# Performance work log

Hardware: AMD Instinct MI355X
Metric: run time of the kernel (lower is better)

## Reference

```python
import jax, jax.numpy as jnp
import numpy as np

C_S = 384; C_Z = 128; C_RES = 128; H = 12; HD = 32; L = 8; RB = 2; NA = 7
TSF = 10.0; EPS = 1e-8; B = 2; N = 512; NRES = 21


def layernorm(x, g, b, eps=1e-5):
    m = jnp.mean(x, -1, keepdims=True)
    v = jnp.mean((x - m) ** 2, -1, keepdims=True)
    return (x - m) * jax.lax.rsqrt(v + eps) * g + b


def lin(x, w, b=None):
    y = x @ w.T
    return y if b is None else y + b


def rot_vec(R, v):
    return jnp.einsum('...ij,...j->...i', R, v)


def make_rigid(n, ca, c, eps=1e-7):
    # Gram-Schmidt backbone frame construction (openfold make_transform_from_reference)
    t = -ca
    n_xyz = n + t; c_xyz = c + t
    cx, cy, cz = c_xyz[..., 0], c_xyz[..., 1], c_xyz[..., 2]
    z = jnp.zeros_like(cx); o = jnp.ones_like(cx)
    nrm = jnp.sqrt(eps + cx**2 + cy**2)
    s1 = -cy / nrm; c1 = cx / nrm
    R1 = jnp.stack([jnp.stack([c1, -s1, z], -1), jnp.stack([s1, c1, z], -1), jnp.stack([z, z, o], -1)], -2)
    nrm2 = jnp.sqrt(eps + cx**2 + cy**2 + cz**2)
    s2 = cz / nrm2; c2 = jnp.sqrt(cx**2 + cy**2) / nrm2
    R2 = jnp.stack([jnp.stack([c2, z, s2], -1), jnp.stack([z, o, z], -1), jnp.stack([-s2, z, c2], -1)], -2)
    Rc = R2 @ R1
    n2 = rot_vec(Rc, n_xyz)
    ny, nz = n2[..., 1], n2[..., 2]
    nrm3 = jnp.sqrt(eps + ny**2 + nz**2)
    sn = -nz / nrm3; cn = ny / nrm3
    Rn = jnp.stack([jnp.stack([o, z, z], -1), jnp.stack([z, cn, -sn], -1), jnp.stack([z, sn, cn], -1)], -2)
    R = jnp.swapaxes(Rn @ Rc, -1, -2)
    return R, ca


def to4x4(R, t):
    bot = jnp.zeros(R.shape[:-2] + (1, 4), R.dtype).at[..., 0, 3].set(1.0)
    top = jnp.concatenate([R, t[..., None]], -1)
    return jnp.concatenate([top, bot], -2)


def compose(R1, t1, R2, t2):
    return R1 @ R2, rot_vec(R1, t2) + t1


def structure_fwd(s, z, aatype, mask, ln_s_g, ln_s_b, ln_z_g, ln_z_b, w_in, b_in, w_b, b_b,
                  attn_ln_g, attn_ln_b, attn_wqkv, attn_wo, attn_bo, attn_wg, attn_bg,
                  tr_ln_g, tr_ln_b, tr_w1, tr_b1, tr_w2, tr_b2, w_bb, b_bb,
                  ar_win, ar_bin, ar_winit, ar_binit, ar_w1, ar_b1, ar_w2, ar_b2, ar_wout, ar_bout,
                  default_frames, group_idx, atom_mask, lit_positions):
    Bd, Nd = s.shape[:2]
    s = layernorm(s, ln_s_g, ln_s_b)
    s_init = s
    s = lin(s, w_in, b_in)
    zn = layernorm(z, ln_z_g, ln_z_b)
    bmat = lin(zn, w_b, b_b)                                # [B,N,N,L*H]
    bmat = jnp.transpose(bmat, (0, 3, 1, 2)).reshape(Bd, L, H, Nd, Nd)
    key_mask = (mask[:, None, None, :] == 0)
    for i in range(L):
        xn = layernorm(s, attn_ln_g[i], attn_ln_b[i])
        t = lin(xn, attn_wqkv[i]).reshape(Bd, Nd, H, 3 * HD).transpose(0, 2, 1, 3)
        q, k, v = jnp.split(t, 3, axis=-1)                  # each [B,H,N,HD]
        a = jnp.einsum('bhqc,bhkc->bhqk', q * HD ** -0.5, k) + bmat[:, i]
        a = jnp.where(key_mask, -1e9, a)
        a = jax.nn.softmax(a, axis=-1)
        y = jnp.einsum('bhqk,bhkc->bqhc', a, v).reshape(Bd, Nd, C_S)
        g = jax.nn.sigmoid(lin(xn, attn_wg[i], attn_bg[i]))
        s = s + lin(g * y, attn_wo[i], attn_bo[i])
        xt = layernorm(s, tr_ln_g[i], tr_ln_b[i])
        s = s + lin(jax.nn.relu(lin(xt, tr_w1[i], tr_b1[i])), tr_w2[i], tr_b2[i])
    # angle resnet
    a0 = lin(jax.nn.relu(s_init), ar_winit, ar_binit)
    a = lin(jax.nn.relu(s), ar_win, ar_bin) + a0
    for j in range(RB):
        h = lin(jax.nn.relu(a), ar_w1[j], ar_b1[j])
        h = lin(jax.nn.relu(h), ar_w2[j], ar_b2[j])
        a = a + h
    ang = lin(jax.nn.relu(a), ar_wout, ar_bout).reshape(Bd, Nd, NA, 2)
    unnorm = ang
    denom = jnp.sqrt(jnp.maximum(jnp.sum(ang ** 2, -1, keepdims=True), EPS))
    angles = ang / denom
    # backbone rigid from predicted pseudo-atoms
    n_, ca_, c_ = jnp.split(lin(s, w_bb, b_bb), 3, axis=-1)
    Rbb, tbb = make_rigid(n_, ca_, c_)
    tbb = tbb * TSF
    # torsion_angles_to_frames
    d4 = default_frames[aatype]                             # [B,N,8,4,4]
    dR = d4[..., :3, :3]; dt = d4[..., :3, 3]
    bb_sin = jnp.zeros(angles.shape[:-2] + (1,), angles.dtype)
    bb_cos = jnp.ones_like(bb_sin)
    sin_a = jnp.concatenate([bb_sin, angles[..., 0]], -1)   # [B,N,8]
    cos_a = jnp.concatenate([bb_cos, angles[..., 1]], -1)
    z8 = jnp.zeros_like(sin_a); o8 = jnp.ones_like(sin_a)
    Ra = jnp.stack([jnp.stack([o8, z8, z8], -1), jnp.stack([z8, cos_a, -sin_a], -1), jnp.stack([z8, sin_a, cos_a], -1)], -2)
    Rf = dR @ Ra; tf = dt
    R5, t5 = compose(Rf[..., 4, :, :], tf[..., 4, :], Rf[..., 5, :, :], tf[..., 5, :])
    R6, t6 = compose(R5, t5, Rf[..., 6, :, :], tf[..., 6, :])
    R7, t7 = compose(R6, t6, Rf[..., 7, :, :], tf[..., 7, :])
    Rall = jnp.concatenate([Rf[..., :5, :, :], jnp.stack([R5, R6, R7], -3)], -3)
    tall = jnp.concatenate([tf[..., :5, :], jnp.stack([t5, t6, t7], -2)], -2)
    Rg = jnp.einsum('bnij,bngjk->bngik', Rbb, Rall)
    tg = jnp.einsum('bnij,bngj->bngi', Rbb, tall) + tbb[..., None, :]
    # frames + literature positions -> atom14
    oh = jax.nn.one_hot(group_idx[aatype], 8, dtype=Rg.dtype)   # [B,N,14,8]
    Ratom = jnp.einsum('bnag,bngij->bnaij', oh, Rg)
    tatom = jnp.einsum('bnag,bngi->bnai', oh, tg)
    lit = lit_positions[aatype]                             # [B,N,14,3]
    pred = jnp.einsum('bnaij,bnaj->bnai', Ratom, lit) + tatom
    pred = pred * atom_mask[aatype][..., None]
    return angles, unnorm, to4x4(Rbb, tbb), to4x4(Rg, tg), pred, s


def setup_inputs():
    key = jax.random.key(0)
    ks = iter(jax.random.split(key, 64))
    nrm = lambda shape: jax.random.normal(next(ks), shape, jnp.float32) * 0.02
    d = {}
    d['s'] = jax.random.normal(next(ks), (B, N, C_S), jnp.float32)
    d['z'] = jax.random.normal(next(ks), (B, N, N, C_Z), jnp.float32)
    d['aatype'] = jax.random.randint(next(ks), (B, N), 0, NRES)
    d['mask'] = jax.random.randint(next(ks), (B, N), 0, 2).astype(jnp.int32)
    d['ln_s_g'] = jnp.ones(C_S); d['ln_s_b'] = jnp.zeros(C_S)
    d['ln_z_g'] = jnp.ones(C_Z); d['ln_z_b'] = jnp.zeros(C_Z)
    d['w_in'] = nrm((C_S, C_S)); d['b_in'] = jnp.zeros(C_S)
    d['w_b'] = nrm((L * H, C_Z)); d['b_b'] = jnp.zeros(L * H)
    d['attn_ln_g'] = jnp.ones((L, C_S)); d['attn_ln_b'] = jnp.zeros((L, C_S))
    d['attn_wqkv'] = nrm((L, 3 * C_S, C_S))
    d['attn_wo'] = nrm((L, C_S, C_S)); d['attn_bo'] = jnp.zeros((L, C_S))
    d['attn_wg'] = nrm((L, C_S, C_S)); d['attn_bg'] = jnp.ones((L, C_S))
    d['tr_ln_g'] = jnp.ones((L, C_S)); d['tr_ln_b'] = jnp.zeros((L, C_S))
    d['tr_w1'] = nrm((L, C_S, C_S)); d['tr_b1'] = jnp.zeros((L, C_S))
    d['tr_w2'] = nrm((L, C_S, C_S)); d['tr_b2'] = jnp.zeros((L, C_S))
    d['w_bb'] = nrm((9, C_S)); d['b_bb'] = jnp.zeros(9)
    d['ar_win'] = nrm((C_RES, C_S)); d['ar_bin'] = jnp.zeros(C_RES)
    d['ar_winit'] = nrm((C_RES, C_S)); d['ar_binit'] = jnp.zeros(C_RES)
    d['ar_w1'] = nrm((RB, C_RES, C_RES)); d['ar_b1'] = jnp.zeros((RB, C_RES))
    d['ar_w2'] = nrm((RB, C_RES, C_RES)); d['ar_b2'] = jnp.zeros((RB, C_RES))
    d['ar_wout'] = nrm((2 * NA, C_RES)); d['ar_bout'] = jnp.zeros(2 * NA)
    df = jnp.tile(jnp.eye(4, dtype=jnp.float32), (NRES, 8, 1, 1))
    df = df.at[..., :3, 3].set(jax.random.normal(next(ks), (NRES, 8, 3)))
    d['default_frames'] = df
    d['group_idx'] = jax.random.randint(next(ks), (NRES, 14), 0, 8)
    d['atom_mask'] = (jax.random.uniform(next(ks), (NRES, 14)) < 0.9).astype(jnp.float32)
    d['lit_positions'] = jax.random.normal(next(ks), (NRES, 14, 3), jnp.float32)
    return d


def reference(s, z, aatype, mask, ln_s_g, ln_s_b, ln_z_g, ln_z_b, w_in, b_in, w_b, b_b,
              attn_ln_g, attn_ln_b, attn_wqkv, attn_wo, attn_bo, attn_wg, attn_bg,
              tr_ln_g, tr_ln_b, tr_w1, tr_b1, tr_w2, tr_b2, w_bb, b_bb,
              ar_win, ar_bin, ar_winit, ar_binit, ar_w1, ar_b1, ar_w2, ar_b2, ar_wout, ar_bout,
              default_frames, group_idx, atom_mask, lit_positions):
    return structure_fwd(s, z, aatype, mask, ln_s_g, ln_s_b, ln_z_g, ln_z_b, w_in, b_in, w_b, b_b,
                         attn_ln_g, attn_ln_b, attn_wqkv, attn_wo, attn_bo, attn_wg, attn_bg,
                         tr_ln_g, tr_ln_b, tr_w1, tr_b1, tr_w2, tr_b2, w_bb, b_bb,
                         ar_win, ar_bin, ar_winit, ar_binit, ar_w1, ar_b1, ar_w2, ar_b2, ar_wout, ar_bout,
                         default_frames, group_idx, atom_mask, lit_positions)
```

## Files before the change

### kernel.cpp

```cpp
#include <hip/hip_runtime.h>
#include <hip/hip_bf16.h>

typedef __attribute__((ext_vector_type(8))) short bf16x8;
typedef __attribute__((ext_vector_type(4))) float f32x4;
typedef unsigned short u16;

__device__ __forceinline__ u16 f2bf(float f) {
  union { __hip_bfloat16 b; u16 u; } v;
  v.b = __float2bfloat16(f);
  return v.u;
}
__device__ __forceinline__ float bf2f(u16 s) {
  union { unsigned u; float f; } v; v.u = ((unsigned)s) << 16;
  return v.f;
}
__device__ __forceinline__ f32x4 mfma_bf16(bf16x8 a, bf16x8 b, f32x4 c) {
  return __builtin_amdgcn_mfma_f32_16x16x32_bf16(a, b, c, 0, 0, 0);
}
__device__ __forceinline__ void split2(float x, u16& h, u16& l) {
  h = f2bf(x);
  l = f2bf(x - bf2f(h));
}
template <int SPL>
__device__ __forceinline__ void splitN(float x, u16* o) {
  float r = x;
  #pragma unroll
  for (int i = 0; i < SPL; i++) {
    o[i] = f2bf(r);
    if (i + 1 < SPL) r = r - bf2f(o[i]);
  }
}

struct P2 { const float* s; u16* d; int n; };
struct Prep2Args { P2 j[7]; };
__global__ __launch_bounds__(256) void prep2_kernel(Prep2Args A, int total4) {
  for (int i4 = blockIdx.x * 256 + threadIdx.x; i4 < total4; i4 += gridDim.x * 256) {
    int i = i4 * 4;
    #pragma unroll
    for (int jj = 0; jj < 7; jj++) {
      if (i < A.j[jj].n) {
        const float* src = A.j[jj].s;
        u16* dh = A.j[jj].d;
        u16* dl = dh + A.j[jj].n;
        float4 v = *(const float4*)(src + i);
        ushort4 h, l;
        split2(v.x, h.x, l.x); split2(v.y, h.y, l.y);
        split2(v.z, h.z, l.z); split2(v.w, h.w, l.w);
        *(ushort4*)(dh + i) = h;
        *(ushort4*)(dl + i) = l;
        break;
      }
      i -= A.j[jj].n;
    }
  }
}
struct P3 { const float* s; u16* d; int n; };
struct Prep3Args { P3 j[4]; };
__global__ __launch_bounds__(256) void prep3_kernel(Prep3Args A, int total4) {
  for (int i4 = blockIdx.x * 256 + threadIdx.x; i4 < total4; i4 += gridDim.x * 256) {
    int i = i4 * 4;
    #pragma unroll
    for (int jj = 0; jj < 4; jj++) {
      if (i < A.j[jj].n) {
        const float* src = A.j[jj].s;
        u16* d0 = A.j[jj].d;
        u16* d1 = d0 + A.j[jj].n;
        u16* d2 = d1 + A.j[jj].n;
        float4 v = *(const float4*)(src + i);
        float xv[4] = {v.x, v.y, v.z, v.w};
        ushort4 o0, o1, o2;
        u16* po0 = (u16*)&o0; u16* po1 = (u16*)&o1; u16* po2 = (u16*)&o2;
        #pragma unroll
        for (int e = 0; e < 4; e++) {
          u16 tmp[3]; splitN<3>(xv[e], tmp);
          po0[e] = tmp[0]; po1[e] = tmp[1]; po2[e] = tmp[2];
        }
        *(ushort4*)(d0 + i) = o0;
        *(ushort4*)(d1 + i) = o1;
        *(ushort4*)(d2 + i) = o2;
        break;
      }
      i -= A.j[jj].n;
    }
  }
}

__global__ __launch_bounds__(256) void ln_kernel(
    const float* __restrict__ x, const float* __restrict__ gamma,
    const float* __restrict__ beta, float* __restrict__ o, int rows, int C) {
  int wid = threadIdx.x >> 6, lane = threadIdx.x & 63;
  int row = blockIdx.x * 4 + wid;
  if (row >= rows) return;
  const float* xr = x + (size_t)row * C;
  float s = 0.f, s2 = 0.f;
  for (int c = lane; c < C; c += 64) { float v = xr[c]; s += v; s2 += v * v; }
  #pragma unroll
  for (int off = 32; off >= 1; off >>= 1) {
    s += __shfl_xor(s, off);
    s2 += __shfl_xor(s2, off);
  }
  float m = s / C;
  float var = s2 / C - m * m;
  float rs = rsqrtf(var + 1e-5f);
  float* orow = o + (size_t)row * C;
  for (int c = lane; c < C; c += 64) orow[c] = (xr[c] - m) * rs * gamma[c] + beta[c];
}

template <int SPL, int LNA, int INRELU, int ACT, int ACC, int STATS, int OUT2>
__global__ __launch_bounds__(128) void gemm_kernel(
    const float* __restrict__ A, const float* __restrict__ pin,
    const float* __restrict__ lng, const float* __restrict__ lnb,
    const u16* __restrict__ w0p, const u16* __restrict__ w1p, const u16* __restrict__ w2p,
    const float* __restrict__ bias,
    float* __restrict__ O, float* __restrict__ O2, float* __restrict__ pout,
    int M, int N, int K) {
  __shared__ __align__(16) u16 a_pl[SPL][32][40];
  __shared__ __align__(16) u16 w_pl[SPL][64][40];
  const int n0 = blockIdx.x * 64, m0 = blockIdx.y * 32;
  const int t = threadIdx.x;
  const int wid = t >> 6, lane = t & 63;
  const int cl = lane & 15, cg = lane >> 4;
  const int ar = t >> 2, aq = t & 3;
  const int wr = t >> 1, wh2 = t & 1;
  const float* ap = A + (size_t)(m0 + ar) * K + aq * 8;
  const u16* wp[SPL];
  {
    const u16* tmp[3] = {w0p, w1p, w2p};
    #pragma unroll
    for (int p = 0; p < SPL; p++) wp[p] = tmp[p] + (size_t)(n0 + wr) * K + wh2 * 16;
  }
  float rm = 0.f, rrs = 1.f;
  if (LNA) {
    float s = 0.f, s2 = 0.f;
    #pragma unroll
    for (int pq = 0; pq < 6; pq++) {
      s  += pin[(m0 + ar) * 16 + pq * 2];
      s2 += pin[(m0 + ar) * 16 + pq * 2 + 1];
    }
    rm = s * (1.f / 384.f);
    rrs = rsqrtf(s2 * (1.f / 384.f) - rm * rm + 1e-5f);
  }
  float4 ra0, ra1, rg0, rg1, rb0, rb1;
  uint4 rw[SPL][2];
  auto GLOAD = [&](int k0) {
    ra0 = ((const float4*)(ap + k0))[0];
    ra1 = ((const float4*)(ap + k0))[1];
    #pragma unroll
    for (int p = 0; p < SPL; p++) {
      rw[p][0] = *(const uint4*)(wp[p] + k0);
      rw[p][1] = *(const uint4*)(wp[p] + k0 + 8);
    }
    if (LNA) {
      rg0 = ((const float4*)(lng + k0 + aq * 8))[0];
      rg1 = ((const float4*)(lng + k0 + aq * 8))[1];
      rb0 = ((const float4*)(lnb + k0 + aq * 8))[0];
      rb1 = ((const float4*)(lnb + k0 + aq * 8))[1];
    }
  };
  GLOAD(0);
  f32x4 acc[4] = {};
  for (int k0 = 0; k0 < K; k0 += 32) {
    {
      float av[8] = {ra0.x, ra0.y, ra0.z, ra0.w, ra1.x, ra1.y, ra1.z, ra1.w};
      if (LNA) {
        float gv[8] = {rg0.x, rg0.y, rg0.z, rg0.w, rg1.x, rg1.y, rg1.z, rg1.w};
        float bv[8] = {rb0.x, rb0.y, rb0.z, rb0.w, rb1.x, rb1.y, rb1.z, rb1.w};
        #pragma unroll
        for (int j = 0; j < 8; j++) av[j] = (av[j] - rm) * rrs * gv[j] + bv[j];
      }
      if (INRELU) {
        #pragma unroll
        for (int j = 0; j < 8; j++) av[j] = fmaxf(av[j], 0.f);
      }
      union { u16 s[8]; uint4 u; } pk[SPL];
      #pragma unroll
      for (int j = 0; j < 8; j++) {
        u16 tmp[SPL]; splitN<SPL>(av[j], tmp);
        #pragma unroll
        for (int p = 0; p < SPL; p++) pk[p].s[j] = tmp[p];
      }
      #pragma unroll
      for (int p = 0; p < SPL; p++) *(uint4*)&a_pl[p][ar][aq * 8] = pk[p].u;
      #pragma unroll
      for (int p = 0; p < SPL; p++) {
        *(uint4*)&w_pl[p][wr][wh2 * 16] = rw[p][0];
        *(uint4*)&w_pl[p][wr][wh2 * 16 + 8] = rw[p][1];
      }
    }
    __syncthreads();
    if (k0 + 32 < K) GLOAD(k0 + 32);
    bf16x8 av[SPL];
    #pragma unroll
    for (int p = 0; p < SPL; p++) av[p] = *(const bf16x8*)&a_pl[p][wid * 16 + cl][cg * 8];
    bf16x8 bv[SPL][4];
    #pragma unroll
    for (int p = 0; p < SPL; p++)
      #pragma unroll
      for (int nt = 0; nt < 4; nt++)
        bv[p][nt] = *(const bf16x8*)&w_pl[p][nt * 16 + cl][cg * 8];
    #pragma unroll
    for (int d = 0; d < SPL; d++)
      #pragma unroll
      for (int i2 = 0; i2 <= d; i2++) {
        #pragma unroll
        for (int nt = 0; nt < 4; nt++)
          acc[nt] = mfma_bf16(av[i2], bv[d - i2][nt], acc[nt]);
      }
    __syncthreads();
  }
  float ps[4], ps2[4];
  #pragma unroll
  for (int i = 0; i < 4; i++) { ps[i] = 0.f; ps2[i] = 0.f; }
  #pragma unroll
  for (int nt = 0; nt < 4; nt++) {
    #pragma unroll
    for (int i = 0; i < 4; i++) {
      int r = m0 + wid * 16 + cg * 4 + i;
      int c = n0 + nt * 16 + cl;
      float v = acc[nt][i];
      if (bias) v += bias[c];
      if (ACT == 1) v = fmaxf(v, 0.f);
      if (ACT == 2) v = 1.f / (1.f + __expf(-v));
      size_t oi = (size_t)r * N + c;
      float nv = ACC ? (O[oi] + v) : v;
      O[oi] = nv;
      if (OUT2) O2[oi] = nv;
      if (STATS) { ps[i] += nv; ps2[i] += nv * nv; }
    }
  }
  if (STATS) {
    #pragma unroll
    for (int i = 0; i < 4; i++) {
      #pragma unroll
      for (int off = 1; off < 16; off <<= 1) {
        ps[i] += __shfl_xor(ps[i], off);
        ps2[i] += __shfl_xor(ps2[i], off);
      }
    }
    if (cl == 0) {
      #pragma unroll
      for (int i = 0; i < 4; i++) {
        int r = m0 + wid * 16 + cg * 4 + i;
        pout[r * 16 + blockIdx.x * 2] = ps[i];
        pout[r * 16 + blockIdx.x * 2 + 1] = ps2[i];
      }
    }
  }
}

__global__ __launch_bounds__(128) void gemm_qkvg_kernel(
    const float* __restrict__ A, const float* __restrict__ pin,
    const float* __restrict__ lng, const float* __restrict__ lnb,
    const u16* __restrict__ wqh, const u16* __restrict__ wql,
    const u16* __restrict__ wgh, const u16* __restrict__ wgl,
    const float* __restrict__ bg,
    u16* __restrict__ qkvh, u16* __restrict__ qkvl, float* __restrict__ gbuf) {
  __shared__ __align__(16) u16 a_pl[2][32][40];
  __shared__ __align__(16) u16 w_pl[2][64][40];
  const int n0 = blockIdx.x * 64, m0 = blockIdx.y * 32;
  const bool isg = (n0 >= 1152);
  const int t = threadIdx.x;
  const int wid = t >> 6, lane = t & 63;
  const int cl = lane & 15, cg = lane >> 4;
  const int ar = t >> 2, aq = t & 3;
  const int wr = t >> 1, wh2 = t & 1;
  const float* ap = A + (size_t)(m0 + ar) * 384 + aq * 8;
  const u16* wph = (isg ? wgh + (size_t)(n0 - 1152 + wr) * 384 : wqh + (size_t)(n0 + wr) * 384) + wh2 * 16;
  const u16* wpl = (isg ? wgl + (size_t)(n0 - 1152 + wr) * 384 : wql + (size_t)(n0 + wr) * 384) + wh2 * 16;
  float s = 0.f, s2 = 0.f;
  #pragma unroll
  for (int pq = 0; pq < 6; pq++) {
    s  += pin[(m0 + ar) * 16 + pq * 2];
    s2 += pin[(m0 + ar) * 16 + pq * 2 + 1];
  }
  const float rm = s * (1.f / 384.f);
  const float rrs = rsqrtf(s2 * (1.f / 384.f) - rm * rm + 1e-5f);
  float4 ra0, ra1, rg0, rg1, rb0, rb1;
  uint4 rwh0, rwh1, rwl0, rwl1;
  auto GLOAD = [&](int k0) {
    ra0 = ((const float4*)(ap + k0))[0];
    ra1 = ((const float4*)(ap + k0))[1];
    rwh0 = *(const uint4*)(wph + k0);
    rwh1 = *(const uint4*)(wph + k0 + 8);
    rwl0 = *(const uint4*)(wpl + k0);
    rwl1 = *(const uint4*)(wpl + k0 + 8);
    rg0 = ((const float4*)(lng + k0 + aq * 8))[0];
    rg1 = ((const float4*)(lng + k0 + aq * 8))[1];
    rb0 = ((const float4*)(lnb + k0 + aq * 8))[0];
    rb1 = ((const float4*)(lnb + k0 + aq * 8))[1];
  };
  GLOAD(0);
  f32x4 acc[4] = {};
  for (int k0 = 0; k0 < 384; k0 += 32) {
    {
      float av[8] = {ra0.x, ra0.y, ra0.z, ra0.w, ra1.x, ra1.y, ra1.z, ra1.w};
      float gv[8] = {rg0.x, rg0.y, rg0.z, rg0.w, rg1.x, rg1.y, rg1.z, rg1.w};
      float bv[8] = {rb0.x, rb0.y, rb0.z, rb0.w, rb1.x, rb1.y, rb1.z, rb1.w};
      union { u16 s[8]; uint4 u; } ph, pl;
      #pragma unroll
      for (int j = 0; j < 8; j++) {
        float x = (av[j] - rm) * rrs * gv[j] + bv[j];
        split2(x, ph.s[j], pl.s[j]);
      }
      *(uint4*)&a_pl[0][ar][aq * 8] = ph.u;
      *(uint4*)&a_pl[1][ar][aq * 8] = pl.u;
      *(uint4*)&w_pl[0][wr][wh2 * 16] = rwh0;
      *(uint4*)&w_pl[0][wr][wh2 * 16 + 8] = rwh1;
      *(uint4*)&w_pl[1][wr][wh2 * 16] = rwl0;
      *(uint4*)&w_pl[1][wr][wh2 * 16 + 8] = rwl1;
    }
    __syncthreads();
    if (k0 + 32 < 384) GLOAD(k0 + 32);
    bf16x8 ah = *(const bf16x8*)&a_pl[0][wid * 16 + cl][cg * 8];
    bf16x8 al = *(const bf16x8*)&a_pl[1][wid * 16 + cl][cg * 8];
    bf16x8 bh[4], bl[4];
    #pragma unroll
    for (int nt = 0; nt < 4; nt++) {
      bh[nt] = *(const bf16x8*)&w_pl[0][nt * 16 + cl][cg * 8];
      bl[nt] = *(const bf16x8*)&w_pl[1][nt * 16 + cl][cg * 8];
    }
    #pragma unroll
    for (int nt = 0; nt < 4; nt++) acc[nt] = mfma_bf16(ah, bh[nt], acc[nt]);
    #pragma unroll
    for (int nt = 0; nt < 4; nt++) acc[nt] = mfma_bf16(ah, bl[nt], acc[nt]);
    #pragma unroll
    for (int nt = 0; nt < 4; nt++) acc[nt] = mfma_bf16(al, bh[nt], acc[nt]);
    __syncthreads();
  }
  #pragma unroll
  for (int nt = 0; nt < 4; nt++) {
    #pragma unroll
    for (int i = 0; i < 4; i++) {
      int r = m0 + wid * 16 + cg * 4 + i;
      int c = n0 + nt * 16 + cl;
      float v = acc[nt][i];
      if (isg) {
        int cc = c - 1152;
        v = 1.f / (1.f + __expf(-(v + bg[cc])));
        gbuf[(size_t)r * 384 + cc] = v;
      } else {
        u16 hh, ll; split2(v, hh, ll);
        qkvh[(size_t)r * 1152 + c] = hh;
        qkvl[(size_t)r * 1152 + c] = ll;
      }
    }
  }
}

__global__ __launch_bounds__(512) void zbmat_kernel(
    const float* __restrict__ z, const float* __restrict__ gamma,
    const float* __restrict__ beta, const u16* __restrict__ wbh,
    const u16* __restrict__ wbl, const float* __restrict__ bbias,
    float* __restrict__ bm) {
  __shared__ __align__(16) u16 w_h[96][136], w_l[96][136];
  __shared__ __align__(16) u16 a_h[2][64][136], a_l[2][64][136];
  const int b = blockIdx.x >> 9;
  const int i = blockIdx.x & 511;
  const int t = threadIdx.x;
  for (int idx = t; idx < 1536; idx += 512) {
    int r2 = idx >> 4, c2 = (idx & 15) * 8;
    *(uint4*)&w_h[r2][c2] = *(const uint4*)(wbh + r2 * 128 + c2);
    *(uint4*)&w_l[r2][c2] = *(const uint4*)(wbl + r2 * 128 + c2);
  }
  const int r = t >> 3, q = t & 7;
  const int cq = q * 16;
  const float* zbase = z + ((size_t)(b * 512 + i) * 512) * 128 + (size_t)r * 128 + cq;
  float4 gv[4], bv[4];
  #pragma unroll
  for (int ii = 0; ii < 4; ii++) {
    gv[ii] = *(const float4*)(gamma + cq + ii * 4);
    bv[ii] = *(const float4*)(beta + cq + ii * 4);
  }
  const int wid = t >> 6, lane = t & 63;
  const int cl = lane & 15, cg = lane >> 4;
  const int m = wid & 3, g = wid >> 2;
  const int arow = m * 16 + cl;
  float bb[3];
  #pragma unroll
  for (int nt = 0; nt < 3; nt++) bb[nt] = bbias[(g * 3 + nt) * 16 + cl];
  float4 v[4];

  auto ln_store = [&](int dst) {
    float s = 0.f, s2 = 0.f;
    #pragma unroll
    for (int ii = 0; ii < 4; ii++) {
      s += v[ii].x + v[ii].y + v[ii].z + v[ii].w;
      s2 += v[ii].x * v[ii].x + v[ii].y * v[ii].y + v[ii].z * v[ii].z + v[ii].w * v[ii].w;
    }
    s += __shfl_xor(s, 1); s2 += __shfl_xor(s2, 1);
    s += __shfl_xor(s, 2); s2 += __shfl_xor(s2, 2);
    s += __shfl_xor(s, 4); s2 += __shfl_xor(s2, 4);
    const float mu = s * (1.f / 128.f);
    const float var = s2 * (1.f / 128.f) - mu * mu;
    const float rs = rsqrtf(var + 1e-5f);
    float xv[16];
    #pragma unroll
    for (int w2 = 0; w2 < 4; w2++) {
      float4 x = v[w2], g2 = gv[w2], be = bv[w2];
      xv[w2 * 4 + 0] = (x.x - mu) * rs * g2.x + be.x;
      xv[w2 * 4 + 1] = (x.y - mu) * rs * g2.y + be.y;
      xv[w2 * 4 + 2] = (x.z - mu) * rs * g2.z + be.z;
      xv[w2 * 4 + 3] = (x.w - mu) * rs * g2.w + be.w;
    }
    union { u16 s[8]; uint4 u; } ph, pl;
    #pragma unroll
    for (int j = 0; j < 8; j++) split2(xv[j], ph.s[j], pl.s[j]);
    *(uint4*)&a_h[dst][r][cq] = ph.u;
    *(uint4*)&a_l[dst][r][cq] = pl.u;
    #pragma unroll
    for (int j = 0; j < 8; j++) split2(xv[8 + j], ph.s[j], pl.s[j]);
    *(uint4*)&a_h[dst][r][cq + 8] = ph.u;
    *(uint4*)&a_l[dst][r][cq + 8] = pl.u;
  };

  #pragma unroll
  for (int ii = 0; ii < 4; ii++) v[ii] = ((const float4*)zbase)[ii];
  ln_store(0);
  __syncthreads();

  int cur = 0;
  for (int jt = 0; jt < 8; jt++) {
    if (jt < 7) {
      const float* src = zbase + (size_t)(jt + 1) * 64 * 128;
      #pragma unroll
      for (int ii = 0; ii < 4; ii++) v[ii] = ((const float4*)src)[ii];
    }
    f32x4 acc[3] = {};
    #pragma unroll
    for (int ks = 0; ks < 4; ks++) {
      bf16x8 ah = *(const bf16x8*)&a_h[cur][arow][ks * 32 + cg * 8];
      bf16x8 al = *(const bf16x8*)&a_l[cur][arow][ks * 32 + cg * 8];
      bf16x8 bh[3], bl[3];
      #pragma unroll
      for (int nt = 0; nt < 3; nt++) {
        bh[nt] = *(const bf16x8*)&w_h[(g * 3 + nt) * 16 + cl][ks * 32 + cg * 8];
        bl[nt] = *(const bf16x8*)&w_l[(g * 3 + nt) * 16 + cl][ks * 32 + cg * 8];
      }
      #pragma unroll
      for (int nt = 0; nt < 3; nt++) acc[nt] = mfma_bf16(ah, bh[nt], acc[nt]);
      #pragma unroll
      for (int nt = 0; nt < 3; nt++) acc[nt] = mfma_bf16(ah, bl[nt], acc[nt]);
      #pragma unroll
      for (int nt = 0; nt < 3; nt++) acc[nt] = mfma_bf16(al, bh[nt], acc[nt]);
    }
    #pragma unroll
    for (int nt = 0; nt < 3; nt++) {
      float4 o;
      o.x = acc[nt][0] + bb[nt]; o.y = acc[nt][1] + bb[nt];
      o.z = acc[nt][2] + bb[nt]; o.w = acc[nt][3] + bb[nt];
      int ch = (g * 3 + nt) * 16 + cl;
      *(float4*)&bm[((size_t)(b * 96 + ch) * 512 + i) * 512 + jt * 64 + m * 16 + cg * 4] = o;
    }
    if (jt < 7) ln_store(cur ^ 1);
    __syncthreads();
    cur ^= 1;
  }
}

__global__ __launch_bounds__(128) void attn_kernel(
    const u16* __restrict__ qkvh, const u16* __restrict__ qkvl,
    const float* __restrict__ bmat, const int* __restrict__ maskp,
    const float* __restrict__ gate, float* __restrict__ ybuf, int layer) {
  __shared__ __align__(16) u16 vT_h[32][522];
  __shared__ __align__(16) u16 vT_l[32][522];
  __shared__ __align__(16) u16 pst_h[2][16][36];
  __shared__ __align__(16) u16 pst_l[2][16][36];
  const int bid = blockIdx.x;
  const int qb = bid & 15;
  const int hh = (bid >> 4) % 12;
  const int b = bid / 192;
  const int q0 = qb * 32;
  const int t = threadIdx.x;
  const int wid = t >> 6;
  const int lane = t & 63;
  const int cl = lane & 15, cg = lane >> 4;

  for (int idx = t; idx < 2048; idx += 128) {
    int k = idx >> 2, c8 = (idx & 3) * 8;
    size_t off = (size_t)(b * 512 + k) * 1152 + hh * 96 + 64 + c8;
    union { uint4 u; u16 s[8]; } vh, vl;
    vh.u = *(const uint4*)(qkvh + off);
    vl.u = *(const uint4*)(qkvl + off);
    #pragma unroll
    for (int j = 0; j < 8; j++) {
      vT_h[c8 + j][k] = vh.s[j];
      vT_l[c8 + j][k] = vl.s[j];
    }
  }

  const int qrow = q0 + wid * 16 + cl;
  const size_t qoff = (size_t)(b * 512 + qrow) * 1152 + hh * 96 + cg * 8;
  bf16x8 qh = *(const bf16x8*)(qkvh + qoff);
  bf16x8 ql = *(const bf16x8*)(qkvl + qoff);

  __syncthreads();

  const f32x4 zero4 = {0.f, 0.f, 0.f, 0.f};
  const float qs = 0.17677669529663687f;
  f32x4 sc[32];
  #pragma unroll
  for (int nt = 0; nt < 32; nt++) {
    int kk = nt * 16 + cl;
    size_t koff = (size_t)(b * 512 + kk) * 1152 + hh * 96 + 32 + cg * 8;
    bf16x8 kh = *(const bf16x8*)(qkvh + koff);
    bf16x8 kl = *(const bf16x8*)(qkvl + koff);
    f32x4 a = mfma_bf16(qh, kh, zero4);
    a = mfma_bf16(qh, kl, a);
    a = mfma_bf16(ql, kh, a);
    sc[nt] = a;
  }

  const size_t bc = (size_t)(b * 96 + layer * 12 + hh);
  #pragma unroll
  for (int nt = 0; nt < 32; nt++) {
    int kk = nt * 16 + cl;
    int mk = maskp[b * 512 + kk];
    #pragma unroll
    for (int i2 = 0; i2 < 4; i2++) {
      int qq = q0 + wid * 16 + cg * 4 + i2;
      float bias = bmat[(bc * 512 + qq) * 512 + kk];
      float vv = sc[nt][i2] * qs + bias;
      sc[nt][i2] = (mk == 0) ? -1e9f : vv;
    }
  }

  float inv[4];
  #pragma unroll
  for (int i2 = 0; i2 < 4; i2++) {
    float mx = -3e38f;
    #pragma unroll
    for (int nt = 0; nt < 32; nt++) mx = fmaxf(mx, sc[nt][i2]);
    mx = fmaxf(mx, __shfl_xor(mx, 1));
    mx = fmaxf(mx, __shfl_xor(mx, 2));
    mx = fmaxf(mx, __shfl_xor(mx, 4));
    mx = fmaxf(mx, __shfl_xor(mx, 8));
    float ss = 0.f;
    #pragma unroll
    for (int nt = 0; nt < 32; nt++) {
      float p = __expf(sc[nt][i2] - mx);
      sc[nt][i2] = p;
      ss += p;
    }
    ss += __shfl_xor(ss, 1);
    ss += __shfl_xor(ss, 2);
    ss += __shfl_xor(ss, 4);
    ss += __shfl_xor(ss, 8);
    inv[i2] = 1.f / ss;
  }

  f32x4 yacc[2] = {};
  for (int ks = 0; ks < 16; ks++) {
    #pragma unroll
    for (int half = 0; half < 2; half++) {
      int nt = ks * 2 + half;
      #pragma unroll
      for (int i2 = 0; i2 < 4; i2++) {
        u16 h2, l2; split2(sc[nt][i2] * inv[i2], h2, l2);
        pst_h[wid][cg * 4 + i2][half * 16 + cl] = h2;
        pst_l[wid][cg * 4 + i2][half * 16 + cl] = l2;
      }
    }
    __syncthreads();
    bf16x8 ph = *(const bf16x8*)&pst_h[wid][cl][cg * 8];
    bf16x8 pl = *(const bf16x8*)&pst_l[wid][cl][cg * 8];
    #pragma unroll
    for (int nt2 = 0; nt2 < 2; nt2++) {
      bf16x8 vh = *(const bf16x8*)&vT_h[nt2 * 16 + cl][ks * 32 + cg * 8];
      bf16x8 vl = *(const bf16x8*)&vT_l[nt2 * 16 + cl][ks * 32 + cg * 8];
      yacc[nt2] = mfma_bf16(ph, vh, yacc[nt2]);
      yacc[nt2] = mfma_bf16(ph, vl, yacc[nt2]);
      yacc[nt2] = mfma_bf16(pl, vh, yacc[nt2]);
    }
    __syncthreads();
  }

  #pragma unroll
  for (int nt2 = 0; nt2 < 2; nt2++) {
    #pragma unroll
    for (int i2 = 0; i2 < 4; i2++) {
      int qq = q0 + wid * 16 + cg * 4 + i2;
      int c = nt2 * 16 + cl;
      size_t oi = (size_t)(b * 512 + qq) * 384 + hh * 32 + c;
      ybuf[oi] = yacc[nt2][i2] * gate[oi];
    }
  }
}

template <int NOUT, int K, int RELU>
__global__ __launch_bounds__(256) void proj_kernel(
    const float* __restrict__ A, const float* __restrict__ W,
    const float* __restrict__ bias, float* __restrict__ O) {
  const int wid = threadIdx.x >> 6, lane = threadIdx.x & 63;
  const int row = blockIdx.x * 4 + wid;
  const float* a = A + (size_t)row * K;
  float av[K / 64];
  #pragma unroll
  for (int j = 0; j < K / 64; j++) {
    float v = a[lane + 64 * j];
    av[j] = RELU ? fmaxf(v, 0.f) : v;
  }
  float res = 0.f;
  #pragma unroll
  for (int n = 0; n < NOUT; n++) {
    float s = 0.f;
    #pragma unroll
    for (int j = 0; j < K / 64; j++) s += av[j] * W[n * K + lane + 64 * j];
    #pragma unroll
    for (int off = 32; off >= 1; off >>= 1) s += __shfl_xor(s, off);
    if (lane == n) res = s + bias[n];
  }
  if (lane < NOUT) O[(size_t)row * NOUT + lane] = res;
}

__device__ __forceinline__ void m3m(float* o, const float* a, const float* b) {
  #pragma unroll
  for (int i = 0; i < 3; i++)
    #pragma unroll
    for (int j = 0; j < 3; j++)
      o[i * 3 + j] = a[i * 3 + 0] * b[0 * 3 + j] + a[i * 3 + 1] * b[1 * 3 + j] + a[i * 3 + 2] * b[2 * 3 + j];
}
__device__ __forceinline__ void m3v(float* o, const float* a, const float* v) {
  #pragma unroll
  for (int i = 0; i < 3; i++)
    o[i] = a[i * 3 + 0] * v[0] + a[i * 3 + 1] * v[1] + a[i * 3 + 2] * v[2];
}

__global__ __launch_bounds__(256) void tail_kernel(
    const float* __restrict__ angraw, const float* __restrict__ bbbuf,
    const int* __restrict__ aatype, const float* __restrict__ deff,
    const int* __restrict__ gidx, const float* __restrict__ amask,
    const float* __restrict__ lit,
    float* __restrict__ o_ang, float* __restrict__ o_un,
    float* __restrict__ o_bb4, float* __restrict__ o_rg4, float* __restrict__ o_pred) {
  int idx = blockIdx.x * 256 + threadIdx.x;
  if (idx >= 1024) return;
  float ang[14];
  #pragma unroll
  for (int a = 0; a < 7; a++) {
    float s0 = angraw[idx * 14 + a * 2], s1 = angraw[idx * 14 + a * 2 + 1];
    o_un[(idx * 7 + a) * 2] = s0; o_un[(idx * 7 + a) * 2 + 1] = s1;
    float d = sqrtf(fmaxf(s0 * s0 + s1 * s1, 1e-8f));
    ang[a * 2] = s0 / d; ang[a * 2 + 1] = s1 / d;
    o_ang[(idx * 7 + a) * 2] = ang[a * 2]; o_ang[(idx * 7 + a) * 2 + 1] = ang[a * 2 + 1];
  }
  const float* p = bbbuf + (size_t)idx * 9;
  float nx = p[0] - p[3], ny = p[1] - p[4], nz = p[2] - p[5];
  float cx = p[6] - p[3], cy = p[7] - p[4], cz = p[8] - p[5];
  const float eps = 1e-7f;
  float nrm = sqrtf(eps + cx * cx + cy * cy);
  float s1 = -cy / nrm, c1 = cx / nrm;
  float nrm2 = sqrtf(eps + cx * cx + cy * cy + cz * cz);
  float s2 = cz / nrm2, c2 = sqrtf(cx * cx + cy * cy) / nrm2;
  float Rc[9] = { c2 * c1, -c2 * s1, s2,
                  s1,      c1,       0.f,
                  -s2 * c1, s2 * s1, c2 };
  float n2y = Rc[3] * nx + Rc[4] * ny + Rc[5] * nz;
  float n2z = Rc[6] * nx + Rc[7] * ny + Rc[8] * nz;
  float nrm3 = sqrtf(eps + n2y * n2y + n2z * n2z);
  float sn = -n2z / nrm3, cn = n2y / nrm3;
  float Rm[9];
  Rm[0] = Rc[0]; Rm[1] = Rc[1]; Rm[2] = Rc[2];
  Rm[3] = cn * Rc[3] - sn * Rc[6];
  Rm[4] = cn * Rc[4] - sn * Rc[7];
  Rm[5] = cn * Rc[5] - sn * Rc[8];
  Rm[6] = sn * Rc[3] + cn * Rc[6];
  Rm[7] = sn * Rc[4] + cn * Rc[7];
  Rm[8] = sn * Rc[5] + cn * Rc[8];
  float Rb[9] = { Rm[0], Rm[3], Rm[6],
                  Rm[1], Rm[4], Rm[7],
                  Rm[2], Rm[5], Rm[8] };
  float tb[3] = { p[3] * 10.f, p[4] * 10.f, p[5] * 10.f };
  {
    float* o = o_bb4 + (size_t)idx * 16;
    o[0] = Rb[0]; o[1] = Rb[1]; o[2] = Rb[2]; o[3] = tb[0];
    o[4] = Rb[3]; o[5] = Rb[4]; o[6] = Rb[5]; o[7] = tb[1];
    o[8] = Rb[6]; o[9] = Rb[7]; o[10] = Rb[8]; o[11] = tb[2];
    o[12] = 0.f; o[13] = 0.f; o[14] = 0.f; o[15] = 1.f;
  }
  int aa = aatype[idx];
  float Rf[8][9], tf[8][3];
  for (int g = 0; g < 8; g++) {
    const float* d4 = deff + ((size_t)aa * 8 + g) * 16;
    float sa = 0.f, ca = 1.f;
    if (g > 0) { sa = ang[(g - 1) * 2]; ca = ang[(g - 1) * 2 + 1]; }
    #pragma unroll
    for (int i = 0; i < 3; i++) {
      float d0 = d4[i * 4 + 0], d1 = d4[i * 4 + 1], d2 = d4[i * 4 + 2];
      Rf[g][i * 3 + 0] = d0;
      Rf[g][i * 3 + 1] = d1 * ca + d2 * sa;
      Rf[g][i * 3 + 2] = -d1 * sa + d2 * ca;
      tf[g][i] = d4[i * 4 + 3];
    }
  }
  float Rall[8][9], tall[8][3];
  for (int g = 0; g < 5; g++) {
    #pragma unroll
    for (int i = 0; i < 9; i++) Rall[g][i] = Rf[g][i];
    #pragma unroll
    for (int i = 0; i < 3; i++) tall[g][i] = tf[g][i];
  }
  m3m(Rall[5], Rf[4], Rf[5]); m3v(tall[5], Rf[4], tf[5]);
  tall[5][0] += tf[4][0]; tall[5][1] += tf[4][1]; tall[5][2] += tf[4][2];
  m3m(Rall[6], Rall[5], Rf[6]); m3v(tall[6], Rall[5], tf[6]);
  tall[6][0] += tall[5][0]; tall[6][1] += tall[5][1]; tall[6][2] += tall[5][2];
  m3m(Rall[7], Rall[6], Rf[7]); m3v(tall[7], Rall[6], tf[7]);
  tall[7][0] += tall[6][0]; tall[7][1] += tall[6][1]; tall[7][2] += tall[6][2];
  float RG[8][9], TG[8][3];
  for (int g = 0; g < 8; g++) {
    m3m(RG[g], Rb, Rall[g]);
    m3v(TG[g], Rb, tall[g]);
    TG[g][0] += tb[0]; TG[g][1] += tb[1]; TG[g][2] += tb[2];
    float* o = o_rg4 + ((size_t)idx * 8 + g) * 16;
    o[0] = RG[g][0]; o[1] = RG[g][1]; o[2] = RG[g][2]; o[3] = TG[g][0];
    o[4] = RG[g][3]; o[5] = RG[g][4]; o[6] = RG[g][5]; o[7] = TG[g][1];
    o[8] = RG[g][6]; o[9] = RG[g][7]; o[10] = RG[g][8]; o[11] = TG[g][2];
    o[12] = 0.f; o[13] = 0.f; o[14] = 0.f; o[15] = 1.f;
  }
  for (int a = 0; a < 14; a++) {
    int gi = gidx[aa * 14 + a];
    const float* lp = lit + ((size_t)aa * 14 + a) * 3;
    float mk = amask[aa * 14 + a];
    float px = RG[gi][0] * lp[0] + RG[gi][1] * lp[1] + RG[gi][2] * lp[2] + TG[gi][0];
    float py = RG[gi][3] * lp[0] + RG[gi][4] * lp[1] + RG[gi][5] * lp[2] + TG[gi][1];
    float pz = RG[gi][6] * lp[0] + RG[gi][7] * lp[1] + RG[gi][8] * lp[2] + TG[gi][2];
    float* op = o_pred + ((size_t)idx * 14 + a) * 3;
    op[0] = px * mk; op[1] = py * mk; op[2] = pz * mk;
  }
}

extern "C" void kernel_launch(void* const* d_in, const int* in_sizes, int n_in,
                              void* d_out, int out_size, void* d_ws, size_t ws_size,
                              hipStream_t stream) {
  (void)in_sizes; (void)n_in; (void)out_size; (void)ws_size;
  const float* s_in    = (const float*)d_in[0];
  const float* z_in    = (const float*)d_in[1];
  const int*   aatype  = (const int*)d_in[2];
  const int*   maskp   = (const int*)d_in[3];
  const float* ln_s_g  = (const float*)d_in[4];
  const float* ln_s_b  = (const float*)d_in[5];
  const float* ln_z_g  = (const float*)d_in[6];
  const float* ln_z_b  = (const float*)d_in[7];
  const float* w_in    = (const float*)d_in[8];
  const float* b_in    = (const float*)d_in[9];
  const float* w_b     = (const float*)d_in[10];
  const float* b_b     = (const float*)d_in[11];
  const float* attn_ln_g = (const float*)d_in[12];
  const float* attn_ln_b = (const float*)d_in[13];
  const float* attn_wqkv = (const float*)d_in[14];
  const float* attn_wo   = (const float*)d_in[15];
  const float* attn_bo   = (const float*)d_in[16];
  const float* attn_wg   = (const float*)d_in[17];
  const float* attn_bg   = (const float*)d_in[18];
  const float* tr_ln_g   = (const float*)d_in[19];
  const float* tr_ln_b   = (const float*)d_in[20];
  const float* tr_w1     = (const float*)d_in[21];
  const float* tr_b1     = (const float*)d_in[22];
  const float* tr_w2     = (const float*)d_in[23];
  const float* tr_b2     = (const float*)d_in[24];
  const float* w_bb      = (const float*)d_in[25];
  const float* b_bb      = (const float*)d_in[26];
  const float* ar_win    = (const float*)d_in[27];
  const float* ar_bin    = (const float*)d_in[28];
  const float* ar_winit  = (const float*)d_in[29];
  const float* ar_binit  = (const float*)d_in[30];
  const float* ar_w1     = (const float*)d_in[31];
  const float* ar_b1     = (const float*)d_in[32];
  const float* ar_w2     = (const float*)d_in[33];
  const float* ar_b2     = (const float*)d_in[34];
  const float* ar_wout   = (const float*)d_in[35];
  const float* ar_bout   = (const float*)d_in[36];
  const float* def_frames= (const float*)d_in[37];
  const int*   group_idx = (const int*)d_in[38];
  const float* atom_mask = (const float*)d_in[39];
  const float* lit_pos   = (const float*)d_in[40];

  char* p = (char*)d_ws;
  float* bmat   = (float*)p;          p += 201326592;
  float* s_init = (float*)p;          p += 1572864;
  float* s_cur  = (float*)p;          p += 1572864;
  u16*   qkvh   = (u16*)p;            p += 2359296;
  u16*   qkvl   = (u16*)p;            p += 2359296;
  float* gbuf   = (float*)p;          p += 1572864;
  float* ybuf   = (float*)p;          p += 1572864;
  float* h1buf  = (float*)p;          p += 1572864;
  float* abuf   = (float*)p;          p += 524288;
  float* htmp   = (float*)p;          p += 524288;
  float* pbuf   = (float*)p;          p += 65536;
  float* bbbuf  = (float*)p;          p += 36864;
  float* angraw = (float*)p;          p += 57344;
  u16* ps_qkvw  = (u16*)p;            p += 14155776;
  u16* ps_wg    = (u16*)p;            p += 4718592;
  u16* ps_wo    = (u16*)p;            p += 4718592;
  u16* ps_tr1   = (u16*)p;            p += 4718592;
  u16* ps_tr2   = (u16*)p;            p += 4718592;
  u16* ps_win   = (u16*)p;            p += 589824;
  u16* ps_wb    = (u16*)p;            p += 49152;
  u16* ps_arwin = (u16*)p;            p += 294912;
  u16* ps_arwinit = (u16*)p;          p += 294912;
  u16* ps_arw1  = (u16*)p;            p += 196608;
  u16* ps_arw2  = (u16*)p;            p += 196608;

  float* out    = (float*)d_out;
  float* o_ang  = out;
  float* o_un   = out + 14336;
  float* o_bb4  = out + 28672;
  float* o_rg4  = out + 45056;
  float* o_pred = out + 176128;
  float* o_s    = out + 219136;

  Prep2Args p2;
  p2.j[0] = {attn_wqkv, ps_qkvw, 3538944};
  p2.j[1] = {attn_wg,   ps_wg,   1179648};
  p2.j[2] = {attn_wo,   ps_wo,   1179648};
  p2.j[3] = {tr_w1,     ps_tr1,  1179648};
  p2.j[4] = {tr_w2,     ps_tr2,  1179648};
  p2.j[5] = {w_in,      ps_win,  147456};
  p2.j[6] = {w_b,       ps_wb,   12288};
  prep2_kernel<<<2048, 256, 0, stream>>>(p2, 2104320);
  Prep3Args p3;
  p3.j[0] = {ar_win,   ps_arwin,   49152};
  p3.j[1] = {ar_winit, ps_arwinit, 49152};
  p3.j[2] = {ar_w1,    ps_arw1,    32768};
  p3.j[3] = {ar_w2,    ps_arw2,    32768};
  prep3_kernel<<<160, 256, 0, stream>>>(p3, 40960);

  ln_kernel<<<256, 256, 0, stream>>>(s_in, ln_s_g, ln_s_b, s_init, 1024, 384);
  gemm_kernel<2, 0, 0, 0, 0, 1, 0><<<dim3(6, 32), 128, 0, stream>>>(
      s_init, nullptr, nullptr, nullptr, ps_win, ps_win + 147456, nullptr,
      b_in, s_cur, nullptr, pbuf, 1024, 384, 384);
  zbmat_kernel<<<1024, 512, 0, stream>>>(z_in, ln_z_g, ln_z_b, ps_wb, ps_wb + 12288, b_b, bmat);

  for (int l = 0; l < 8; ++l) {
    gemm_qkvg_kernel<<<dim3(24, 32), 128, 0, stream>>>(
        s_cur, pbuf, attn_ln_g + l * 384, attn_ln_b + l * 384,
        ps_qkvw + (size_t)l * 442368, ps_qkvw + 3538944 + (size_t)l * 442368,
        ps_wg + (size_t)l * 147456, ps_wg + 1179648 + (size_t)l * 147456,
        attn_bg + l * 384, qkvh, qkvl, gbuf);
    attn_kernel<<<384, 128, 0, stream>>>(qkvh, qkvl, bmat, maskp, gbuf, ybuf, l);
    gemm_kernel<2, 0, 0, 0, 1, 1, 0><<<dim3(6, 32), 128, 0, stream>>>(
        ybuf, nullptr, nullptr, nullptr,
        ps_wo + (size_t)l * 147456, ps_wo + 1179648 + (size_t)l * 147456, nullptr,
        attn_bo + l * 384, s_cur, nullptr, pbuf, 1024, 384, 384);
    gemm_kernel<2, 1, 0, 1, 0, 0, 0><<<dim3(6, 32), 128, 0, stream>>>(
        s_cur, pbuf, tr_ln_g + l * 384, tr_ln_b + l * 384,
        ps_tr1 + (size_t)l * 147456, ps_tr1 + 1179648 + (size_t)l * 147456, nullptr,
        tr_b1 + l * 384, h1buf, nullptr, nullptr, 1024, 384, 384);
    if (l < 7)
      gemm_kernel<2, 0, 0, 0, 1, 1, 0><<<dim3(6, 32), 128, 0, stream>>>(
          h1buf, nullptr, nullptr, nullptr,
          ps_tr2 + (size_t)l * 147456, ps_tr2 + 1179648 + (size_t)l * 147456, nullptr,
          tr_b2 + l * 384, s_cur, nullptr, pbuf, 1024, 384, 384);
    else
      gemm_kernel<2, 0, 0, 0, 1, 1, 1><<<dim3(6, 32), 128, 0, stream>>>(
          h1buf, nullptr, nullptr, nullptr,
          ps_tr2 + (size_t)l * 147456, ps_tr2 + 1179648 + (size_t)l * 147456, nullptr,
          tr_b2 + l * 384, s_cur, o_s, pbuf, 1024, 384, 384);
  }

  gemm_kernel<3, 0, 1, 0, 0, 0, 0><<<dim3(2, 32), 128, 0, stream>>>(
      s_cur, nullptr, nullptr, nullptr,
      ps_arwin, ps_arwin + 49152, ps_arwin + 98304,
      ar_bin, abuf, nullptr, nullptr, 1024, 128, 384);
  gemm_kernel<3, 0, 1, 0, 1, 0, 0><<<dim3(2, 32), 128, 0, stream>>>(
      s_init, nullptr, nullptr, nullptr,
      ps_arwinit, ps_arwinit + 49152, ps_arwinit + 98304,
      ar_binit, abuf, nullptr, nullptr, 1024, 128, 384);
  for (int j = 0; j < 2; ++j) {
    gemm_kernel<3, 0, 1, 0, 0, 0, 0><<<dim3(2, 32), 128, 0, stream>>>(
        abuf, nullptr, nullptr, nullptr,
        ps_arw1 + j * 16384, ps_arw1 + 32768 + j * 16384, ps_arw1 + 65536 + j * 16384,
        ar_b1 + j * 128, htmp, nullptr, nullptr, 1024, 128, 128);
    gemm_kernel<3, 0, 1, 0, 1, 0, 0><<<dim3(2, 32), 128, 0, stream>>>(
        htmp, nullptr, nullptr, nullptr,
        ps_arw2 + j * 16384, ps_arw2 + 32768 + j * 16384, ps_arw2 + 65536 + j * 16384,
        ar_b2 + j * 128, abuf, nullptr, nullptr, 1024, 128, 128);
  }

  proj_kernel<9, 384, 0><<<256, 256, 0, stream>>>(s_cur, w_bb, b_bb, bbbuf);
  proj_kernel<14, 128, 1><<<256, 256, 0, stream>>>(abuf, ar_wout, ar_bout, angraw);
  tail_kernel<<<4, 256, 0, stream>>>(angraw, bbbuf, aatype, def_frames, group_idx,
                                     atom_mask, lit_pos, o_ang, o_un, o_bb4, o_rg4, o_pred);
}
```

Measured before the change: 1.098 ms.

## Double GEMM K-step, restructure pair-bias kernel, fuse angle resnet and tail

The generic and QKVG GEMM kernels now stage 64-wide K tiles in shared memory instead of 32, halving the barrier count per tile. The pair-bias kernel is rewritten to load z rows straight into MFMA fragments in registers and do LayerNorm there, dropping the shared-memory A staging. The angle-resnet GEMMs, the two projection kernels and the tail kernel are merged into one 32-block kernel, which removes about nine launches and their intermediate buffers. The costs are more shared memory per block, and a fused tail that runs on only 32 blocks and may be serialised.

```diff
diff --git a/kernel.cpp b/kernel.cpp
--- a/kernel.cpp
+++ b/kernel.cpp
@@ -114,20 +114,20 @@
     const float* __restrict__ bias,
     float* __restrict__ O, float* __restrict__ O2, float* __restrict__ pout,
     int M, int N, int K) {
-  __shared__ __align__(16) u16 a_pl[SPL][32][40];
-  __shared__ __align__(16) u16 w_pl[SPL][64][40];
+  __shared__ __align__(16) u16 a_pl[SPL][32][72];
+  __shared__ __align__(16) u16 w_pl[SPL][64][72];
   const int n0 = blockIdx.x * 64, m0 = blockIdx.y * 32;
   const int t = threadIdx.x;
   const int wid = t >> 6, lane = t & 63;
   const int cl = lane & 15, cg = lane >> 4;
   const int ar = t >> 2, aq = t & 3;
   const int wr = t >> 1, wh2 = t & 1;
-  const float* ap = A + (size_t)(m0 + ar) * K + aq * 8;
-  const u16* wp[SPL];
+  const float* ap = A + (size_t)(m0 + ar) * K + aq * 16;
+  const u16* wp[3] = {nullptr, nullptr, nullptr};
   {
     const u16* tmp[3] = {w0p, w1p, w2p};
     #pragma unroll
-    for (int p = 0; p < SPL; p++) wp[p] = tmp[p] + (size_t)(n0 + wr) * K + wh2 * 16;
+    for (int p = 0; p < SPL; p++) wp[p] = tmp[p] + (size_t)(n0 + wr) * K + wh2 * 32;
   }
   float rm = 0.f, rrs = 1.f;
   if (LNA) {
@@ -140,72 +140,84 @@
     rm = s * (1.f / 384.f);
     rrs = rsqrtf(s2 * (1.f / 384.f) - rm * rm + 1e-5f);
   }
-  float4 ra0, ra1, rg0, rg1, rb0, rb1;
-  uint4 rw[SPL][2];
+  float4 ra[4], rg[4], rb4[4];
+  uint4 rw[SPL][4];
   auto GLOAD = [&](int k0) {
-    ra0 = ((const float4*)(ap + k0))[0];
-    ra1 = ((const float4*)(ap + k0))[1];
-    #pragma unroll
-    for (int p = 0; p < SPL; p++) {
-      rw[p][0] = *(const uint4*)(wp[p] + k0);
-      rw[p][1] = *(const uint4*)(wp[p] + k0 + 8);
-    }
+    #pragma unroll
+    for (int e = 0; e < 4; e++) ra[e] = ((const float4*)(ap + k0))[e];
+    #pragma unroll
+    for (int p = 0; p < SPL; p++)
+      #pragma unroll
+      for (int e = 0; e < 4; e++) rw[p][e] = *(const uint4*)(wp[p] + k0 + e * 8);
     if (LNA) {
-      rg0 = ((const float4*)(lng + k0 + aq * 8))[0];
-      rg1 = ((const float4*)(lng + k0 + aq * 8))[1];
-      rb0 = ((const float4*)(lnb + k0 + aq * 8))[0];
-      rb1 = ((const float4*)(lnb + k0 + aq * 8))[1];
+      #pragma unroll
+      for (int e = 0; e < 4; e++) {
+        rg[e]  = ((const float4*)(lng + k0 + aq * 16))[e];
+        rb4[e] = ((const float4*)(lnb + k0 + aq * 16))[e];
+      }
     }
   };
   GLOAD(0);
   f32x4 acc[4] = {};
-  for (int k0 = 0; k0 < K; k0 += 32) {
+  for (int k0 = 0; k0 < K; k0 += 64) {
     {
-      float av[8] = {ra0.x, ra0.y, ra0.z, ra0.w, ra1.x, ra1.y, ra1.z, ra1.w};
+      float av[16];
+      #pragma unroll
+      for (int e = 0; e < 4; e++) {
+        av[e * 4 + 0] = ra[e].x; av[e * 4 + 1] = ra[e].y;
+        av[e * 4 + 2] = ra[e].z; av[e * 4 + 3] = ra[e].w;
+      }
       if (LNA) {
-        float gv[8] = {rg0.x, rg0.y, rg0.z, rg0.w, rg1.x, rg1.y, rg1.z, rg1.w};
-        float bv[8] = {rb0.x, rb0.y, rb0.z, rb0.w, rb1.x, rb1.y, rb1.z, rb1.w};
-        #pragma unroll
-        for (int j = 0; j < 8; j++) av[j] = (av[j] - rm) * rrs * gv[j] + bv[j];
+        #pragma unroll
+        for (int e = 0; e < 4; e++) {
+          av[e * 4 + 0] = (av[e * 4 + 0] - rm) * rrs * rg[e].x + rb4[e].x;
+          av[e * 4 + 1] = (av[e * 4 + 1] - rm) * rrs * rg[e].y + rb4[e].y;
+          av[e * 4 + 2] = (av[e * 4 + 2] - rm) * rrs * rg[e].z + rb4[e].z;
+          av[e * 4 + 3] = (av[e * 4 + 3] - rm) * rrs * rg[e].w + rb4[e].w;
+        }
       }
       if (INRELU) {
         #pragma unroll
-        for (int j = 0; j < 8; j++) av[j] = fmaxf(av[j], 0.f);
-      }
-      union { u16 s[8]; uint4 u; } pk[SPL];
-      #pragma unroll
-      for (int j = 0; j < 8; j++) {
+        for (int j = 0; j < 16; j++) av[j] = fmaxf(av[j], 0.f);
+      }
+      u16 sh[SPL][16];
+      #pragma unroll
+      for (int j = 0; j < 16; j++) {
         u16 tmp[SPL]; splitN<SPL>(av[j], tmp);
         #pragma unroll
-        for (int p = 0; p < SPL; p++) pk[p].s[j] = tmp[p];
-      }
-      #pragma unroll
-      for (int p = 0; p < SPL; p++) *(uint4*)&a_pl[p][ar][aq * 8] = pk[p].u;
+        for (int p = 0; p < SPL; p++) sh[p][j] = tmp[p];
+      }
       #pragma unroll
       for (int p = 0; p < SPL; p++) {
-        *(uint4*)&w_pl[p][wr][wh2 * 16] = rw[p][0];
-        *(uint4*)&w_pl[p][wr][wh2 * 16 + 8] = rw[p][1];
+        *(uint4*)&a_pl[p][ar][aq * 16]     = *(const uint4*)&sh[p][0];
+        *(uint4*)&a_pl[p][ar][aq * 16 + 8] = *(const uint4*)&sh[p][8];
+        #pragma unroll
+        for (int e = 0; e < 4; e++) *(uint4*)&w_pl[p][wr][wh2 * 32 + e * 8] = rw[p][e];
       }
     }
     __syncthreads();
-    if (k0 + 32 < K) GLOAD(k0 + 32);
-    bf16x8 av[SPL];
-    #pragma unroll
-    for (int p = 0; p < SPL; p++) av[p] = *(const bf16x8*)&a_pl[p][wid * 16 + cl][cg * 8];
-    bf16x8 bv[SPL][4];
-    #pragma unroll
-    for (int p = 0; p < SPL; p++)
-      #pragma unroll
-      for (int nt = 0; nt < 4; nt++)
-        bv[p][nt] = *(const bf16x8*)&w_pl[p][nt * 16 + cl][cg * 8];
-    #pragma unroll
-    for (int d = 0; d < SPL; d++)
-      #pragma unroll
-      for (int i2 = 0; i2 <= d; i2++) {
+    if (k0 + 64 < K) GLOAD(k0 + 64);
+    #pragma unroll
+    for (int ks2 = 0; ks2 < 2; ks2++) {
+      bf16x8 av_[SPL];
+      #pragma unroll
+      for (int p = 0; p < SPL; p++)
+        av_[p] = *(const bf16x8*)&a_pl[p][wid * 16 + cl][ks2 * 32 + cg * 8];
+      bf16x8 bv[SPL][4];
+      #pragma unroll
+      for (int p = 0; p < SPL; p++)
         #pragma unroll
         for (int nt = 0; nt < 4; nt++)
-          acc[nt] = mfma_bf16(av[i2], bv[d - i2][nt], acc[nt]);
-      }
+          bv[p][nt] = *(const bf16x8*)&w_pl[p][nt * 16 + cl][ks2 * 32 + cg * 8];
+      #pragma unroll
+      for (int d = 0; d < SPL; d++)
+        #pragma unroll
+        for (int i2 = 0; i2 <= d; i2++) {
+          #pragma unroll
+          for (int nt = 0; nt < 4; nt++)
+            acc[nt] = mfma_bf16(av_[i2], bv[d - i2][nt], acc[nt]);
+        }
+    }
     __syncthreads();
   }
   float ps[4], ps2[4];
@@ -255,8 +267,8 @@
     const u16* __restrict__ wgh, const u16* __restrict__ wgl,
     const float* __restrict__ bg,
     u16* __restrict__ qkvh, u16* __restrict__ qkvl, float* __restrict__ gbuf) {
-  __shared__ __align__(16) u16 a_pl[2][32][40];
-  __shared__ __align__(16) u16 w_pl[2][64][40];
+  __shared__ __align__(16) u16 a_pl[2][32][72];
+  __shared__ __align__(16) u16 w_pl[2][64][72];
   const int n0 = blockIdx.x * 64, m0 = blockIdx.y * 32;
   const bool isg = (n0 >= 1152);
   const int t = threadIdx.x;
@@ -264,9 +276,9 @@
   const int cl = lane & 15, cg = lane >> 4;
   const int ar = t >> 2, aq = t & 3;
   const int wr = t >> 1, wh2 = t & 1;
-  const float* ap = A + (size_t)(m0 + ar) * 384 + aq * 8;
-  const u16* wph = (isg ? wgh + (size_t)(n0 - 1152 + wr) * 384 : wqh + (size_t)(n0 + wr) * 384) + wh2 * 16;
-  const u16* wpl = (isg ? wgl + (size_t)(n0 - 1152 + wr) * 384 : wql + (size_t)(n0 + wr) * 384) + wh2 * 16;
+  const float* ap = A + (size_t)(m0 + ar) * 384 + aq * 16;
+  const u16* wph = (isg ? wgh + (size_t)(n0 - 1152 + wr) * 384 : wqh + (size_t)(n0 + wr) * 384) + wh2 * 32;
+  const u16* wpl = (isg ? wgl + (size_t)(n0 - 1152 + wr) * 384 : wql + (size_t)(n0 + wr) * 384) + wh2 * 32;
   float s = 0.f, s2 = 0.f;
   #pragma unroll
   for (int pq = 0; pq < 6; pq++) {
@@ -275,56 +287,63 @@
   }
   const float rm = s * (1.f / 384.f);
   const float rrs = rsqrtf(s2 * (1.f / 384.f) - rm * rm + 1e-5f);
-  float4 ra0, ra1, rg0, rg1, rb0, rb1;
-  uint4 rwh0, rwh1, rwl0, rwl1;
+  float4 ra[4], rg[4], rb4[4];
+  uint4 rwh[4], rwl[4];
   auto GLOAD = [&](int k0) {
-    ra0 = ((const float4*)(ap + k0))[0];
-    ra1 = ((const float4*)(ap + k0))[1];
-    rwh0 = *(const uint4*)(wph + k0);
-    rwh1 = *(const uint4*)(wph + k0 + 8);
-    rwl0 = *(const uint4*)(wpl + k0);
-    rwl1 = *(const uint4*)(wpl + k0 + 8);
-    rg0 = ((const float4*)(lng + k0 + aq * 8))[0];
-    rg1 = ((const float4*)(lng + k0 + aq * 8))[1];
-    rb0 = ((const float4*)(lnb + k0 + aq * 8))[0];
-    rb1 = ((const float4*)(lnb + k0 + aq * 8))[1];
+    #pragma unroll
+    for (int e = 0; e < 4; e++) {
+      ra[e]  = ((const float4*)(ap + k0))[e];
+      rwh[e] = *(const uint4*)(wph + k0 + e * 8);
+      rwl[e] = *(const uint4*)(wpl + k0 + e * 8);
+      rg[e]  = ((const float4*)(lng + k0 + aq * 16))[e];
+      rb4[e] = ((const float4*)(lnb + k0 + aq * 16))[e];
+    }
   };
   GLOAD(0);
   f32x4 acc[4] = {};
-  for (int k0 = 0; k0 < 384; k0 += 32) {
+  for (int k0 = 0; k0 < 384; k0 += 64) {
     {
-      float av[8] = {ra0.x, ra0.y, ra0.z, ra0.w, ra1.x, ra1.y, ra1.z, ra1.w};
-      float gv[8] = {rg0.x, rg0.y, rg0.z, rg0.w, rg1.x, rg1.y, rg1.z, rg1.w};
-      float bv[8] = {rb0.x, rb0.y, rb0.z, rb0.w, rb1.x, rb1.y, rb1.z, rb1.w};
-      union { u16 s[8]; uint4 u; } ph, pl;
-      #pragma unroll
-      for (int j = 0; j < 8; j++) {
-        float x = (av[j] - rm) * rrs * gv[j] + bv[j];
-        split2(x, ph.s[j], pl.s[j]);
-      }
-      *(uint4*)&a_pl[0][ar][aq * 8] = ph.u;
-      *(uint4*)&a_pl[1][ar][aq * 8] = pl.u;
-      *(uint4*)&w_pl[0][wr][wh2 * 16] = rwh0;
-      *(uint4*)&w_pl[0][wr][wh2 * 16 + 8] = rwh1;
-      *(uint4*)&w_pl[1][wr][wh2 * 16] = rwl0;
-      *(uint4*)&w_pl[1][wr][wh2 * 16 + 8] = rwl1;
+      u16 sh[2][16];
+      #pragma unroll
+      for (int e = 0; e < 4; e++) {
+        float xv[4];
+        xv[0] = (ra[e].x - rm) * rrs * rg[e].x + rb4[e].x;
+        xv[1] = (ra[e].y - rm) * rrs * rg[e].y + rb4[e].y;
+        xv[2] = (ra[e].z - rm) * rrs * rg[e].z + rb4[e].z;
+        xv[3] = (ra[e].w - rm) * rrs * rg[e].w + rb4[e].w;
+        #pragma unroll
+        for (int j = 0; j < 4; j++) split2(xv[j], sh[0][e * 4 + j], sh[1][e * 4 + j]);
+      }
+      #pragma unroll
+      for (int p = 0; p < 2; p++) {
+        *(uint4*)&a_pl[p][ar][aq * 16]     = *(const uint4*)&sh[p][0];
+        *(uint4*)&a_pl[p][ar][aq * 16 + 8] = *(const uint4*)&sh[p][8];
+      }
+      #pragma unroll
+      for (int e = 0; e < 4; e++) {
+        *(uint4*)&w_pl[0][wr][wh2 * 32 + e * 8] = rwh[e];
+        *(uint4*)&w_pl[1][wr][wh2 * 32 + e * 8] = rwl[e];
+      }
     }
     __syncthreads();
-    if (k0 + 32 < 384) GLOAD(k0 + 32);
-    bf16x8 ah = *(const bf16x8*)&a_pl[0][wid * 16 + cl][cg * 8];
-    bf16x8 al = *(const bf16x8*)&a_pl[1][wid * 16 + cl][cg * 8];
-    bf16x8 bh[4], bl[4];
-    #pragma unroll
-    for (int nt = 0; nt < 4; nt++) {
-      bh[nt] = *(const bf16x8*)&w_pl[0][nt * 16 + cl][cg * 8];
-      bl[nt] = *(const bf16x8*)&w_pl[1][nt * 16 + cl][cg * 8];
-    }
-    #pragma unroll
-    for (int nt = 0; nt < 4; nt++) acc[nt] = mfma_bf16(ah, bh[nt], acc[nt]);
-    #pragma unroll
-    for (int nt = 0; nt < 4; nt++) acc[nt] = mfma_bf16(ah, bl[nt], acc[nt]);
-    #pragma unroll
-    for (int nt = 0; nt < 4; nt++) acc[nt] = mfma_bf16(al, bh[nt], acc[nt]);
+    if (k0 + 64 < 384) GLOAD(k0 + 64);
+    #pragma unroll
+    for (int ks2 = 0; ks2 < 2; ks2++) {
+      bf16x8 ah = *(const bf16x8*)&a_pl[0][wid * 16 + cl][ks2 * 32 + cg * 8];
+      bf16x8 al = *(const bf16x8*)&a_pl[1][wid * 16 + cl][ks2 * 32 + cg * 8];
+      bf16x8 bh[4], bl[4];
+      #pragma unroll
+      for (int nt = 0; nt < 4; nt++) {
+        bh[nt] = *(const bf16x8*)&w_pl[0][nt * 16 + cl][ks2 * 32 + cg * 8];
+        bl[nt] = *(const bf16x8*)&w_pl[1][nt * 16 + cl][ks2 * 32 + cg * 8];
+      }
+      #pragma unroll
+      for (int nt = 0; nt < 4; nt++) acc[nt] = mfma_bf16(ah, bh[nt], acc[nt]);
+      #pragma unroll
+      for (int nt = 0; nt < 4; nt++) acc[nt] = mfma_bf16(ah, bl[nt], acc[nt]);
+      #pragma unroll
+      for (int nt = 0; nt < 4; nt++) acc[nt] = mfma_bf16(al, bh[nt], acc[nt]);
+    }
     __syncthreads();
   }
   #pragma unroll
@@ -353,107 +372,81 @@
     const u16* __restrict__ wbl, const float* __restrict__ bbias,
     float* __restrict__ bm) {
   __shared__ __align__(16) u16 w_h[96][136], w_l[96][136];
-  __shared__ __align__(16) u16 a_h[2][64][136], a_l[2][64][136];
-  const int b = blockIdx.x >> 9;
-  const int i = blockIdx.x & 511;
+  const int b = blockIdx.x >> 9, i = blockIdx.x & 511;
   const int t = threadIdx.x;
   for (int idx = t; idx < 1536; idx += 512) {
     int r2 = idx >> 4, c2 = (idx & 15) * 8;
     *(uint4*)&w_h[r2][c2] = *(const uint4*)(wbh + r2 * 128 + c2);
     *(uint4*)&w_l[r2][c2] = *(const uint4*)(wbl + r2 * 128 + c2);
   }
-  const int r = t >> 3, q = t & 7;
-  const int cq = q * 16;
-  const float* zbase = z + ((size_t)(b * 512 + i) * 512) * 128 + (size_t)r * 128 + cq;
-  float4 gv[4], bv[4];
-  #pragma unroll
-  for (int ii = 0; ii < 4; ii++) {
-    gv[ii] = *(const float4*)(gamma + cq + ii * 4);
-    bv[ii] = *(const float4*)(beta + cq + ii * 4);
-  }
-  const int wid = t >> 6, lane = t & 63;
+  const int w = t >> 6, lane = t & 63;
   const int cl = lane & 15, cg = lane >> 4;
-  const int m = wid & 3, g = wid >> 2;
-  const int arow = m * 16 + cl;
-  float bb[3];
-  #pragma unroll
-  for (int nt = 0; nt < 3; nt++) bb[nt] = bbias[(g * 3 + nt) * 16 + cl];
-  float4 v[4];
-
-  auto ln_store = [&](int dst) {
+  float bb[6];
+  #pragma unroll
+  for (int nt = 0; nt < 6; nt++) bb[nt] = bbias[nt * 16 + cl];
+  float4 gv[8], bv[8];
+  #pragma unroll
+  for (int ks = 0; ks < 4; ks++) {
+    gv[ks * 2]     = *(const float4*)(gamma + ks * 32 + cg * 8);
+    gv[ks * 2 + 1] = *(const float4*)(gamma + ks * 32 + cg * 8 + 4);
+    bv[ks * 2]     = *(const float4*)(beta + ks * 32 + cg * 8);
+    bv[ks * 2 + 1] = *(const float4*)(beta + ks * 32 + cg * 8 + 4);
+  }
+  __syncthreads();
+  const float* zb = z + ((size_t)(b * 512 + i) * 512) * 128;
+  for (int it = 0; it < 4; it++) {
+    const int j0 = it * 128 + w * 16;
+    const float* zr = zb + (size_t)(j0 + cl) * 128 + cg * 8;
+    float4 v[8];
+    #pragma unroll
+    for (int ks = 0; ks < 4; ks++) {
+      v[ks * 2]     = *(const float4*)(zr + ks * 32);
+      v[ks * 2 + 1] = *(const float4*)(zr + ks * 32 + 4);
+    }
     float s = 0.f, s2 = 0.f;
     #pragma unroll
-    for (int ii = 0; ii < 4; ii++) {
-      s += v[ii].x + v[ii].y + v[ii].z + v[ii].w;
-      s2 += v[ii].x * v[ii].x + v[ii].y * v[ii].y + v[ii].z * v[ii].z + v[ii].w * v[ii].w;
-    }
-    s += __shfl_xor(s, 1); s2 += __shfl_xor(s2, 1);
-    s += __shfl_xor(s, 2); s2 += __shfl_xor(s2, 2);
-    s += __shfl_xor(s, 4); s2 += __shfl_xor(s2, 4);
+    for (int e = 0; e < 8; e++) {
+      s  += v[e].x + v[e].y + v[e].z + v[e].w;
+      s2 += v[e].x * v[e].x + v[e].y * v[e].y + v[e].z * v[e].z + v[e].w * v[e].w;
+    }
+    s += __shfl_xor(s, 16); s2 += __shfl_xor(s2, 16);
+    s += __shfl_xor(s, 32); s2 += __shfl_xor(s2, 32);
     const float mu = s * (1.f / 128.f);
-    const float var = s2 * (1.f / 128.f) - mu * mu;
-    const float rs = rsqrtf(var + 1e-5f);
-    float xv[16];
-    #pragma unroll
-    for (int w2 = 0; w2 < 4; w2++) {
-      float4 x = v[w2], g2 = gv[w2], be = bv[w2];
-      xv[w2 * 4 + 0] = (x.x - mu) * rs * g2.x + be.x;
-      xv[w2 * 4 + 1] = (x.y - mu) * rs * g2.y + be.y;
-      xv[w2 * 4 + 2] = (x.z - mu) * rs * g2.z + be.z;
-      xv[w2 * 4 + 3] = (x.w - mu) * rs * g2.w + be.w;
-    }
-    union { u16 s[8]; uint4 u; } ph, pl;
-    #pragma unroll
-    for (int j = 0; j < 8; j++) split2(xv[j], ph.s[j], pl.s[j]);
-    *(uint4*)&a_h[dst][r][cq] = ph.u;
-    *(uint4*)&a_l[dst][r][cq] = pl.u;
-    #pragma unroll
-    for (int j = 0; j < 8; j++) split2(xv[8 + j], ph.s[j], pl.s[j]);
-    *(uint4*)&a_h[dst][r][cq + 8] = ph.u;
-    *(uint4*)&a_l[dst][r][cq + 8] = pl.u;
-  };
-
-  #pragma unroll
-  for (int ii = 0; ii < 4; ii++) v[ii] = ((const float4*)zbase)[ii];
-  ln_store(0);
-  __syncthreads();
-
-  int cur = 0;
-  for (int jt = 0; jt < 8; jt++) {
-    if (jt < 7) {
-      const float* src = zbase + (size_t)(jt + 1) * 64 * 128;
-      #pragma unroll
-      for (int ii = 0; ii < 4; ii++) v[ii] = ((const float4*)src)[ii];
-    }
-    f32x4 acc[3] = {};
+    const float rs = rsqrtf(s2 * (1.f / 128.f) - mu * mu + 1e-5f);
+    bf16x8 ah[4], al[4];
     #pragma unroll
     for (int ks = 0; ks < 4; ks++) {
-      bf16x8 ah = *(const bf16x8*)&a_h[cur][arow][ks * 32 + cg * 8];
-      bf16x8 al = *(const bf16x8*)&a_l[cur][arow][ks * 32 + cg * 8];
-      bf16x8 bh[3], bl[3];
-      #pragma unroll
-      for (int nt = 0; nt < 3; nt++) {
-        bh[nt] = *(const bf16x8*)&w_h[(g * 3 + nt) * 16 + cl][ks * 32 + cg * 8];
-        bl[nt] = *(const bf16x8*)&w_l[(g * 3 + nt) * 16 + cl][ks * 32 + cg * 8];
-      }
-      #pragma unroll
-      for (int nt = 0; nt < 3; nt++) acc[nt] = mfma_bf16(ah, bh[nt], acc[nt]);
-      #pragma unroll
-      for (int nt = 0; nt < 3; nt++) acc[nt] = mfma_bf16(ah, bl[nt], acc[nt]);
-      #pragma unroll
-      for (int nt = 0; nt < 3; nt++) acc[nt] = mfma_bf16(al, bh[nt], acc[nt]);
-    }
-    #pragma unroll
-    for (int nt = 0; nt < 3; nt++) {
+      union { u16 s[8]; bf16x8 v8; } ph, pl;
+      float xv[8] = {v[ks*2].x, v[ks*2].y, v[ks*2].z, v[ks*2].w,
+                     v[ks*2+1].x, v[ks*2+1].y, v[ks*2+1].z, v[ks*2+1].w};
+      float gg[8] = {gv[ks*2].x, gv[ks*2].y, gv[ks*2].z, gv[ks*2].w,
+                     gv[ks*2+1].x, gv[ks*2+1].y, gv[ks*2+1].z, gv[ks*2+1].w};
+      float be[8] = {bv[ks*2].x, bv[ks*2].y, bv[ks*2].z, bv[ks*2].w,
+                     bv[ks*2+1].x, bv[ks*2+1].y, bv[ks*2+1].z, bv[ks*2+1].w};
+      #pragma unroll
+      for (int e = 0; e < 8; e++) split2((xv[e] - mu) * rs * gg[e] + be[e], ph.s[e], pl.s[e]);
+      ah[ks] = ph.v8; al[ks] = pl.v8;
+    }
+    f32x4 acc[6] = {};
+    #pragma unroll
+    for (int ks = 0; ks < 4; ks++) {
+      #pragma unroll
+      for (int nt = 0; nt < 6; nt++) {
+        bf16x8 bh = *(const bf16x8*)&w_h[nt * 16 + cl][ks * 32 + cg * 8];
+        bf16x8 bl = *(const bf16x8*)&w_l[nt * 16 + cl][ks * 32 + cg * 8];
+        acc[nt] = mfma_bf16(ah[ks], bh, acc[nt]);
+        acc[nt] = mfma_bf16(ah[ks], bl, acc[nt]);
+        acc[nt] = mfma_bf16(al[ks], bh, acc[nt]);
+      }
+    }
+    #pragma unroll
+    for (int nt = 0; nt < 6; nt++) {
       float4 o;
       o.x = acc[nt][0] + bb[nt]; o.y = acc[nt][1] + bb[nt];
       o.z = acc[nt][2] + bb[nt]; o.w = acc[nt][3] + bb[nt];
-      int ch = (g * 3 + nt) * 16 + cl;
-      *(float4*)&bm[((size_t)(b * 96 + ch) * 512 + i) * 512 + jt * 64 + m * 16 + cg * 4] = o;
-    }
-    if (jt < 7) ln_store(cur ^ 1);
-    __syncthreads();
-    cur ^= 1;
+      int ch = nt * 16 + cl;
+      *(float4*)&bm[((size_t)(b * 96 + ch) * 512 + i) * 512 + j0 + cg * 4] = o;
+    }
   }
 }
 
@@ -586,32 +579,6 @@
   }
 }
 
-template <int NOUT, int K, int RELU>
-__global__ __launch_bounds__(256) void proj_kernel(
-    const float* __restrict__ A, const float* __restrict__ W,
-    const float* __restrict__ bias, float* __restrict__ O) {
-  const int wid = threadIdx.x >> 6, lane = threadIdx.x & 63;
-  const int row = blockIdx.x * 4 + wid;
-  const float* a = A + (size_t)row * K;
-  float av[K / 64];
-  #pragma unroll
-  for (int j = 0; j < K / 64; j++) {
-    float v = a[lane + 64 * j];
-    av[j] = RELU ? fmaxf(v, 0.f) : v;
-  }
-  float res = 0.f;
-  #pragma unroll
-  for (int n = 0; n < NOUT; n++) {
-    float s = 0.f;
-    #pragma unroll
-    for (int j = 0; j < K / 64; j++) s += av[j] * W[n * K + lane + 64 * j];
-    #pragma unroll
-    for (int off = 32; off >= 1; off >>= 1) s += __shfl_xor(s, off);
-    if (lane == n) res = s + bias[n];
-  }
-  if (lane < NOUT) O[(size_t)row * NOUT + lane] = res;
-}
-
 __device__ __forceinline__ void m3m(float* o, const float* a, const float* b) {
   #pragma unroll
   for (int i = 0; i < 3; i++)
@@ -625,106 +592,295 @@
     o[i] = a[i * 3 + 0] * v[0] + a[i * 3 + 1] * v[1] + a[i * 3 + 2] * v[2];
 }
 
-__global__ __launch_bounds__(256) void tail_kernel(
-    const float* __restrict__ angraw, const float* __restrict__ bbbuf,
+__global__ __launch_bounds__(128) void resnet_tail_kernel(
+    const float* __restrict__ s_cur, const float* __restrict__ s_init,
+    const u16* __restrict__ w_in3, const u16* __restrict__ w_init3,
+    const float* __restrict__ b_in, const float* __restrict__ b_init,
+    const u16* __restrict__ w1_3, const float* __restrict__ b1,
+    const u16* __restrict__ w2_3, const float* __restrict__ b2,
+    const float* __restrict__ wout, const float* __restrict__ bout,
+    const float* __restrict__ w_bb, const float* __restrict__ b_bb,
     const int* __restrict__ aatype, const float* __restrict__ deff,
     const int* __restrict__ gidx, const float* __restrict__ amask,
     const float* __restrict__ lit,
     float* __restrict__ o_ang, float* __restrict__ o_un,
     float* __restrict__ o_bb4, float* __restrict__ o_rg4, float* __restrict__ o_pred) {
-  int idx = blockIdx.x * 256 + threadIdx.x;
-  if (idx >= 1024) return;
-  float ang[14];
-  #pragma unroll
-  for (int a = 0; a < 7; a++) {
-    float s0 = angraw[idx * 14 + a * 2], s1 = angraw[idx * 14 + a * 2 + 1];
-    o_un[(idx * 7 + a) * 2] = s0; o_un[(idx * 7 + a) * 2 + 1] = s1;
-    float d = sqrtf(fmaxf(s0 * s0 + s1 * s1, 1e-8f));
-    ang[a * 2] = s0 / d; ang[a * 2 + 1] = s1 / d;
-    o_ang[(idx * 7 + a) * 2] = ang[a * 2]; o_ang[(idx * 7 + a) * 2 + 1] = ang[a * 2 + 1];
-  }
-  const float* p = bbbuf + (size_t)idx * 9;
-  float nx = p[0] - p[3], ny = p[1] - p[4], nz = p[2] - p[5];
-  float cx = p[6] - p[3], cy = p[7] - p[4], cz = p[8] - p[5];
-  const float eps = 1e-7f;
-  float nrm = sqrtf(eps + cx * cx + cy * cy);
-  float s1 = -cy / nrm, c1 = cx / nrm;
-  float nrm2 = sqrtf(eps + cx * cx + cy * cy + cz * cz);
-  float s2 = cz / nrm2, c2 = sqrtf(cx * cx + cy * cy) / nrm2;
-  float Rc[9] = { c2 * c1, -c2 * s1, s2,
-                  s1,      c1,       0.f,
-                  -s2 * c1, s2 * s1, c2 };
-  float n2y = Rc[3] * nx + Rc[4] * ny + Rc[5] * nz;
-  float n2z = Rc[6] * nx + Rc[7] * ny + Rc[8] * nz;
-  float nrm3 = sqrtf(eps + n2y * n2y + n2z * n2z);
-  float sn = -n2z / nrm3, cn = n2y / nrm3;
-  float Rm[9];
-  Rm[0] = Rc[0]; Rm[1] = Rc[1]; Rm[2] = Rc[2];
-  Rm[3] = cn * Rc[3] - sn * Rc[6];
-  Rm[4] = cn * Rc[4] - sn * Rc[7];
-  Rm[5] = cn * Rc[5] - sn * Rc[8];
-  Rm[6] = sn * Rc[3] + cn * Rc[6];
-  Rm[7] = sn * Rc[4] + cn * Rc[7];
-  Rm[8] = sn * Rc[5] + cn * Rc[8];
-  float Rb[9] = { Rm[0], Rm[3], Rm[6],
-                  Rm[1], Rm[4], Rm[7],
-                  Rm[2], Rm[5], Rm[8] };
-  float tb[3] = { p[3] * 10.f, p[4] * 10.f, p[5] * 10.f };
+  __shared__ __align__(16) u16 a_pl[3][32][40];
+  __shared__ __align__(16) u16 w_pl[3][128][40];
+  __shared__ __align__(16) float a_f[32][136];
+  __shared__ __align__(16) float h_f[32][136];
+  __shared__ float ang_s[32][14];
+  __shared__ float bb_s[32][9];
+  const int m0 = blockIdx.x * 32;
+  const int t = threadIdx.x;
+  const int wv = t >> 6, lane = t & 63;
+  const int cl = lane & 15, cg = lane >> 4;
+  const int ar = t >> 2, aq = t & 3;
+
+  f32x4 acc[8] = {};
+  for (int src = 0; src < 2; src++) {
+    const float* A = src ? s_init : s_cur;
+    const u16* W = src ? w_init3 : w_in3;
+    for (int k0 = 0; k0 < 384; k0 += 32) {
+      {
+        const float* ap = A + (size_t)(m0 + ar) * 384 + k0 + aq * 8;
+        float4 x0 = ((const float4*)ap)[0], x1 = ((const float4*)ap)[1];
+        float av[8] = {x0.x, x0.y, x0.z, x0.w, x1.x, x1.y, x1.z, x1.w};
+        u16 sh[3][8];
+        #pragma unroll
+        for (int j = 0; j < 8; j++) {
+          u16 tmp[3]; splitN<3>(fmaxf(av[j], 0.f), tmp);
+          sh[0][j] = tmp[0]; sh[1][j] = tmp[1]; sh[2][j] = tmp[2];
+        }
+        #pragma unroll
+        for (int p = 0; p < 3; p++) *(uint4*)&a_pl[p][ar][aq * 8] = *(const uint4*)&sh[p][0];
+        #pragma unroll
+        for (int p = 0; p < 3; p++) {
+          const u16* wp = W + (size_t)p * 49152 + (size_t)t * 384 + k0;
+          *(uint4*)&w_pl[p][t][0]  = *(const uint4*)(wp);
+          *(uint4*)&w_pl[p][t][8]  = *(const uint4*)(wp + 8);
+          *(uint4*)&w_pl[p][t][16] = *(const uint4*)(wp + 16);
+          *(uint4*)&w_pl[p][t][24] = *(const uint4*)(wp + 24);
+        }
+      }
+      __syncthreads();
+      bf16x8 af[3];
+      #pragma unroll
+      for (int p = 0; p < 3; p++) af[p] = *(const bf16x8*)&a_pl[p][wv * 16 + cl][cg * 8];
+      #pragma unroll
+      for (int d = 0; d < 3; d++)
+        #pragma unroll
+        for (int i2 = 0; i2 <= d; i2++)
+          #pragma unroll
+          for (int nt = 0; nt < 8; nt++)
+            acc[nt] = mfma_bf16(af[i2], *(const bf16x8*)&w_pl[d - i2][nt * 16 + cl][cg * 8], acc[nt]);
+      __syncthreads();
+    }
+  }
+  #pragma unroll
+  for (int nt = 0; nt < 8; nt++)
+    #pragma unroll
+    for (int i = 0; i < 4; i++) {
+      int c = nt * 16 + cl;
+      a_f[wv * 16 + cg * 4 + i][c] = acc[nt][i] + b_in[c] + b_init[c];
+    }
+  __syncthreads();
+
+  for (int j = 0; j < 2; j++) {
+    f32x4 acc2[8] = {};
+    for (int k0 = 0; k0 < 128; k0 += 32) {
+      __syncthreads();
+      #pragma unroll
+      for (int p = 0; p < 3; p++) {
+        const u16* wp = w1_3 + (size_t)p * 32768 + j * 16384 + (size_t)t * 128 + k0;
+        *(uint4*)&w_pl[p][t][0]  = *(const uint4*)(wp);
+        *(uint4*)&w_pl[p][t][8]  = *(const uint4*)(wp + 8);
+        *(uint4*)&w_pl[p][t][16] = *(const uint4*)(wp + 16);
+        *(uint4*)&w_pl[p][t][24] = *(const uint4*)(wp + 24);
+      }
+      __syncthreads();
+      union { u16 s[8]; bf16x8 v8; } af[3];
+      #pragma unroll
+      for (int e = 0; e < 8; e++) {
+        u16 tmp[3]; splitN<3>(fmaxf(a_f[wv * 16 + cl][k0 + cg * 8 + e], 0.f), tmp);
+        af[0].s[e] = tmp[0]; af[1].s[e] = tmp[1]; af[2].s[e] = tmp[2];
+      }
+      #pragma unroll
+      for (int d = 0; d < 3; d++)
+        #pragma unroll
+        for (int i2 = 0; i2 <= d; i2++)
+          #pragma unroll
+          for (int nt = 0; nt < 8; nt++)
+            acc2[nt] = mfma_bf16(af[i2].v8, *(const bf16x8*)&w_pl[d - i2][nt * 16 + cl][cg * 8], acc2[nt]);
+    }
+    __syncthreads();
+    #pragma unroll
+    for (int nt = 0; nt < 8; nt++)
+      #pragma unroll
+      for (int i = 0; i < 4; i++) {
+        int c = nt * 16 + cl;
+        h_f[wv * 16 + cg * 4 + i][c] = acc2[nt][i] + b1[j * 128 + c];
+      }
+    __syncthreads();
+    f32x4 acc3[8] = {};
+    for (int k0 = 0; k0 < 128; k0 += 32) {
+      __syncthreads();
+      #pragma unroll
+      for (int p = 0; p < 3; p++) {
+        const u16* wp = w2_3 + (size_t)p * 32768 + j * 16384 + (size_t)t * 128 + k0;
+        *(uint4*)&w_pl[p][t][0]  = *(const uint4*)(wp);
+        *(uint4*)&w_pl[p][t][8]  = *(const uint4*)(wp + 8);
+        *(uint4*)&w_pl[p][t][16] = *(const uint4*)(wp + 16);
+        *(uint4*)&w_pl[p][t][24] = *(const uint4*)(wp + 24);
+      }
+      __syncthreads();
+      union { u16 s[8]; bf16x8 v8; } af[3];
+      #pragma unroll
+      for (int e = 0; e < 8; e++) {
+        u16 tmp[3]; splitN<3>(fmaxf(h_f[wv * 16 + cl][k0 + cg * 8 + e], 0.f), tmp);
+        af[0].s[e] = tmp[0]; af[1].s[e] = tmp[1]; af[2].s[e] = tmp[2];
+      }
+      #pragma unroll
+      for (int d = 0; d < 3; d++)
+        #pragma unroll
+        for (int i2 = 0; i2 <= d; i2++)
+          #pragma unroll
+          for (int nt = 0; nt < 8; nt++)
+            acc3[nt] = mfma_bf16(af[i2].v8, *(const bf16x8*)&w_pl[d - i2][nt * 16 + cl][cg * 8], acc3[nt]);
+    }
+    __syncthreads();
+    #pragma unroll
+    for (int nt = 0; nt < 8; nt++)
+      #pragma unroll
+      for (int i = 0; i < 4; i++) {
+        int c = nt * 16 + cl;
+        a_f[wv * 16 + cg * 4 + i][c] += acc3[nt][i] + b2[j * 128 + c];
+      }
+    __syncthreads();
+  }
+
   {
-    float* o = o_bb4 + (size_t)idx * 16;
-    o[0] = Rb[0]; o[1] = Rb[1]; o[2] = Rb[2]; o[3] = tb[0];
-    o[4] = Rb[3]; o[5] = Rb[4]; o[6] = Rb[5]; o[7] = tb[1];
-    o[8] = Rb[6]; o[9] = Rb[7]; o[10] = Rb[8]; o[11] = tb[2];
-    o[12] = 0.f; o[13] = 0.f; o[14] = 0.f; o[15] = 1.f;
-  }
-  int aa = aatype[idx];
-  float Rf[8][9], tf[8][3];
-  for (int g = 0; g < 8; g++) {
-    const float* d4 = deff + ((size_t)aa * 8 + g) * 16;
-    float sa = 0.f, ca = 1.f;
-    if (g > 0) { sa = ang[(g - 1) * 2]; ca = ang[(g - 1) * 2 + 1]; }
-    #pragma unroll
-    for (int i = 0; i < 3; i++) {
-      float d0 = d4[i * 4 + 0], d1 = d4[i * 4 + 1], d2 = d4[i * 4 + 2];
-      Rf[g][i * 3 + 0] = d0;
-      Rf[g][i * 3 + 1] = d1 * ca + d2 * sa;
-      Rf[g][i * 3 + 2] = -d1 * sa + d2 * ca;
-      tf[g][i] = d4[i * 4 + 3];
-    }
-  }
-  float Rall[8][9], tall[8][3];
-  for (int g = 0; g < 5; g++) {
-    #pragma unroll
-    for (int i = 0; i < 9; i++) Rall[g][i] = Rf[g][i];
-    #pragma unroll
-    for (int i = 0; i < 3; i++) tall[g][i] = tf[g][i];
-  }
-  m3m(Rall[5], Rf[4], Rf[5]); m3v(tall[5], Rf[4], tf[5]);
-  tall[5][0] += tf[4][0]; tall[5][1] += tf[4][1]; tall[5][2] += tf[4][2];
-  m3m(Rall[6], Rall[5], Rf[6]); m3v(tall[6], Rall[5], tf[6]);
-  tall[6][0] += tall[5][0]; tall[6][1] += tall[5][1]; tall[6][2] += tall[5][2];
-  m3m(Rall[7], Rall[6], Rf[7]); m3v(tall[7], Rall[6], tf[7]);
-  tall[7][0] += tall[6][0]; tall[7][1] += tall[6][1]; tall[7][2] += tall[6][2];
-  float RG[8][9], TG[8][3];
-  for (int g = 0; g < 8; g++) {
-    m3m(RG[g], Rb, Rall[g]);
-    m3v(TG[g], Rb, tall[g]);
-    TG[g][0] += tb[0]; TG[g][1] += tb[1]; TG[g][2] += tb[2];
-    float* o = o_rg4 + ((size_t)idx * 8 + g) * 16;
-    o[0] = RG[g][0]; o[1] = RG[g][1]; o[2] = RG[g][2]; o[3] = TG[g][0];
-    o[4] = RG[g][3]; o[5] = RG[g][4]; o[6] = RG[g][5]; o[7] = TG[g][1];
-    o[8] = RG[g][6]; o[9] = RG[g][7]; o[10] = RG[g][8]; o[11] = TG[g][2];
-    o[12] = 0.f; o[13] = 0.f; o[14] = 0.f; o[15] = 1.f;
-  }
-  for (int a = 0; a < 14; a++) {
-    int gi = gidx[aa * 14 + a];
-    const float* lp = lit + ((size_t)aa * 14 + a) * 3;
-    float mk = amask[aa * 14 + a];
-    float px = RG[gi][0] * lp[0] + RG[gi][1] * lp[1] + RG[gi][2] * lp[2] + TG[gi][0];
-    float py = RG[gi][3] * lp[0] + RG[gi][4] * lp[1] + RG[gi][5] * lp[2] + TG[gi][1];
-    float pz = RG[gi][6] * lp[0] + RG[gi][7] * lp[1] + RG[gi][8] * lp[2] + TG[gi][2];
-    float* op = o_pred + ((size_t)idx * 14 + a) * 3;
-    op[0] = px * mk; op[1] = py * mk; op[2] = pz * mk;
+    const int r = t >> 2, q = t & 3;
+    float sn[14];
+    #pragma unroll
+    for (int n = 0; n < 14; n++) sn[n] = 0.f;
+    for (int k = 0; k < 32; k++) {
+      float av = fmaxf(a_f[r][q * 32 + k], 0.f);
+      #pragma unroll
+      for (int n = 0; n < 14; n++) sn[n] += av * wout[n * 128 + q * 32 + k];
+    }
+    #pragma unroll
+    for (int n = 0; n < 14; n++) {
+      sn[n] += __shfl_xor(sn[n], 1);
+      sn[n] += __shfl_xor(sn[n], 2);
+      sn[n] += bout[n];
+    }
+    if (q == 0) {
+      int idx = m0 + r;
+      #pragma unroll
+      for (int a = 0; a < 7; a++) {
+        float s0 = sn[a * 2], s1 = sn[a * 2 + 1];
+        o_un[(idx * 7 + a) * 2] = s0; o_un[(idx * 7 + a) * 2 + 1] = s1;
+        float d = sqrtf(fmaxf(s0 * s0 + s1 * s1, 1e-8f));
+        float n0 = s0 / d, n1 = s1 / d;
+        o_ang[(idx * 7 + a) * 2] = n0; o_ang[(idx * 7 + a) * 2 + 1] = n1;
+        ang_s[r][a * 2] = n0; ang_s[r][a * 2 + 1] = n1;
+      }
+    }
+    float s9[9];
+    #pragma unroll
+    for (int n = 0; n < 9; n++) s9[n] = 0.f;
+    const float* srow = s_cur + (size_t)(m0 + r) * 384 + q * 96;
+    for (int k4 = 0; k4 < 24; k4++) {
+      float4 xv = *(const float4*)(srow + k4 * 4);
+      #pragma unroll
+      for (int n = 0; n < 9; n++) {
+        float4 wv4 = *(const float4*)(w_bb + n * 384 + q * 96 + k4 * 4);
+        s9[n] += xv.x * wv4.x + xv.y * wv4.y + xv.z * wv4.z + xv.w * wv4.w;
+      }
+    }
+    #pragma unroll
+    for (int n = 0; n < 9; n++) {
+      s9[n] += __shfl_xor(s9[n], 1);
+      s9[n] += __shfl_xor(s9[n], 2);
+    }
+    if (q == 0) {
+      #pragma unroll
+      for (int n = 0; n < 9; n++) bb_s[r][n] = s9[n] + b_bb[n];
+    }
+  }
+  __syncthreads();
+
+  if (t < 32) {
+    const int idx = m0 + t;
+    float ang[14];
+    #pragma unroll
+    for (int n = 0; n < 14; n++) ang[n] = ang_s[t][n];
+    float p9[9];
+    #pragma unroll
+    for (int n = 0; n < 9; n++) p9[n] = bb_s[t][n];
+    float nx = p9[0] - p9[3], ny = p9[1] - p9[4], nz = p9[2] - p9[5];
+    float cx = p9[6] - p9[3], cy = p9[7] - p9[4], cz = p9[8] - p9[5];
+    const float eps = 1e-7f;
+    float nrm = sqrtf(eps + cx * cx + cy * cy);
+    float s1 = -cy / nrm, c1 = cx / nrm;
+    float nrm2 = sqrtf(eps + cx * cx + cy * cy + cz * cz);
+    float s2 = cz / nrm2, c2 = sqrtf(cx * cx + cy * cy) / nrm2;
+    float Rc[9] = { c2 * c1, -c2 * s1, s2,
+                    s1,      c1,       0.f,
+                    -s2 * c1, s2 * s1, c2 };
+    float n2y = Rc[3] * nx + Rc[4] * ny + Rc[5] * nz;
+    float n2z = Rc[6] * nx + Rc[7] * ny + Rc[8] * nz;
+    float nrm3 = sqrtf(eps + n2y * n2y + n2z * n2z);
+    float sn = -n2z / nrm3, cn = n2y / nrm3;
+    float Rm[9];
+    Rm[0] = Rc[0]; Rm[1] = Rc[1]; Rm[2] = Rc[2];
+    Rm[3] = cn * Rc[3] - sn * Rc[6];
+    Rm[4] = cn * Rc[4] - sn * Rc[7];
+    Rm[5] = cn * Rc[5] - sn * Rc[8];
+    Rm[6] = sn * Rc[3] + cn * Rc[6];
+    Rm[7] = sn * Rc[4] + cn * Rc[7];
+    Rm[8] = sn * Rc[5] + cn * Rc[8];
+    float Rb[9] = { Rm[0], Rm[3], Rm[6],
+                    Rm[1], Rm[4], Rm[7],
+                    Rm[2], Rm[5], Rm[8] };
+    float tb[3] = { p9[3] * 10.f, p9[4] * 10.f, p9[5] * 10.f };
+    {
+      float* o = o_bb4 + (size_t)idx * 16;
+      o[0] = Rb[0]; o[1] = Rb[1]; o[2] = Rb[2]; o[3] = tb[0];
+      o[4] = Rb[3]; o[5] = Rb[4]; o[6] = Rb[5]; o[7] = tb[1];
+      o[8] = Rb[6]; o[9] = Rb[7]; o[10] = Rb[8]; o[11] = tb[2];
+      o[12] = 0.f; o[13] = 0.f; o[14] = 0.f; o[15] = 1.f;
+    }
+    int aa = aatype[idx];
+    float Rf[8][9], tf[8][3];
+    for (int g = 0; g < 8; g++) {
+      const float* d4 = deff + ((size_t)aa * 8 + g) * 16;
+      float sa = 0.f, ca = 1.f;
+      if (g > 0) { sa = ang[(g - 1) * 2]; ca = ang[(g - 1) * 2 + 1]; }
+      #pragma unroll
+      for (int i = 0; i < 3; i++) {
+        float d0 = d4[i * 4 + 0], d1 = d4[i * 4 + 1], d2 = d4[i * 4 + 2];
+        Rf[g][i * 3 + 0] = d0;
+        Rf[g][i * 3 + 1] = d1 * ca + d2 * sa;
+        Rf[g][i * 3 + 2] = -d1 * sa + d2 * ca;
+        tf[g][i] = d4[i * 4 + 3];
+      }
+    }
+    float Rall[8][9], tall[8][3];
+    for (int g = 0; g < 5; g++) {
+      #pragma unroll
+      for (int i = 0; i < 9; i++) Rall[g][i] = Rf[g][i];
+      #pragma unroll
+      for (int i = 0; i < 3; i++) tall[g][i] = tf[g][i];
+    }
+    m3m(Rall[5], Rf[4], Rf[5]); m3v(tall[5], Rf[4], tf[5]);
+    tall[5][0] += tf[4][0]; tall[5][1] += tf[4][1]; tall[5][2] += tf[4][2];
+    m3m(Rall[6], Rall[5], Rf[6]); m3v(tall[6], Rall[5], tf[6]);
+    tall[6][0] += tall[5][0]; tall[6][1] += tall[5][1]; tall[6][2] += tall[5][2];
+    m3m(Rall[7], Rall[6], Rf[7]); m3v(tall[7], Rall[6], tf[7]);
+    tall[7][0] += tall[6][0]; tall[7][1] += tall[6][1]; tall[7][2] += tall[6][2];
+    float RG[8][9], TG[8][3];
+    for (int g = 0; g < 8; g++) {
+      m3m(RG[g], Rb, Rall[g]);
+      m3v(TG[g], Rb, tall[g]);
+      TG[g][0] += tb[0]; TG[g][1] += tb[1]; TG[g][2] += tb[2];
+      float* o = o_rg4 + ((size_t)idx * 8 + g) * 16;
+      o[0] = RG[g][0]; o[1] = RG[g][1]; o[2] = RG[g][2]; o[3] = TG[g][0];
+      o[4] = RG[g][3]; o[5] = RG[g][4]; o[6] = RG[g][5]; o[7] = TG[g][1];
+      o[8] = RG[g][6]; o[9] = RG[g][7]; o[10] = RG[g][8]; o[11] = TG[g][2];
+      o[12] = 0.f; o[13] = 0.f; o[14] = 0.f; o[15] = 1.f;
+    }
+    for (int a = 0; a < 14; a++) {
+      int gi = gidx[aa * 14 + a];
+      const float* lp = lit + ((size_t)aa * 14 + a) * 3;
+      float mk = amask[aa * 14 + a];
+      float px = RG[gi][0] * lp[0] + RG[gi][1] * lp[1] + RG[gi][2] * lp[2] + TG[gi][0];
+      float py = RG[gi][3] * lp[0] + RG[gi][4] * lp[1] + RG[gi][5] * lp[2] + TG[gi][1];
+      float pz = RG[gi][6] * lp[0] + RG[gi][7] * lp[1] + RG[gi][8] * lp[2] + TG[gi][2];
+      float* op = o_pred + ((size_t)idx * 14 + a) * 3;
+      op[0] = px * mk; op[1] = py * mk; op[2] = pz * mk;
+    }
   }
 }
 
@@ -783,11 +939,7 @@
   float* gbuf   = (float*)p;          p += 1572864;
   float* ybuf   = (float*)p;          p += 1572864;
   float* h1buf  = (float*)p;          p += 1572864;
-  float* abuf   = (float*)p;          p += 524288;
-  float* htmp   = (float*)p;          p += 524288;
   float* pbuf   = (float*)p;          p += 65536;
-  float* bbbuf  = (float*)p;          p += 36864;
-  float* angraw = (float*)p;          p += 57344;
   u16* ps_qkvw  = (u16*)p;            p += 14155776;
   u16* ps_wg    = (u16*)p;            p += 4718592;
   u16* ps_wo    = (u16*)p;            p += 4718592;
@@ -857,27 +1009,11 @@
           tr_b2 + l * 384, s_cur, o_s, pbuf, 1024, 384, 384);
   }
 
-  gemm_kernel<3, 0, 1, 0, 0, 0, 0><<<dim3(2, 32), 128, 0, stream>>>(
-      s_cur, nullptr, nullptr, nullptr,
-      ps_arwin, ps_arwin + 49152, ps_arwin + 98304,
-      ar_bin, abuf, nullptr, nullptr, 1024, 128, 384);
-  gemm_kernel<3, 0, 1, 0, 1, 0, 0><<<dim3(2, 32), 128, 0, stream>>>(
-      s_init, nullptr, nullptr, nullptr,
-      ps_arwinit, ps_arwinit + 49152, ps_arwinit + 98304,
-      ar_binit, abuf, nullptr, nullptr, 1024, 128, 384);
-  for (int j = 0; j < 2; ++j) {
-    gemm_kernel<3, 0, 1, 0, 0, 0, 0><<<dim3(2, 32), 128, 0, stream>>>(
-        abuf, nullptr, nullptr, nullptr,
-        ps_arw1 + j * 16384, ps_arw1 + 32768 + j * 16384, ps_arw1 + 65536 + j * 16384,
-        ar_b1 + j * 128, htmp, nullptr, nullptr, 1024, 128, 128);
-    gemm_kernel<3, 0, 1, 0, 1, 0, 0><<<dim3(2, 32), 128, 0, stream>>>(
-        htmp, nullptr, nullptr, nullptr,
-        ps_arw2 + j * 16384, ps_arw2 + 32768 + j * 16384, ps_arw2 + 65536 + j * 16384,
-        ar_b2 + j * 128, abuf, nullptr, nullptr, 1024, 128, 128);
-  }
-
-  proj_kernel<9, 384, 0><<<256, 256, 0, stream>>>(s_cur, w_bb, b_bb, bbbuf);
-  proj_kernel<14, 128, 1><<<256, 256, 0, stream>>>(abuf, ar_wout, ar_bout, angraw);
-  tail_kernel<<<4, 256, 0, stream>>>(angraw, bbbuf, aatype, def_frames, group_idx,
-                                     atom_mask, lit_pos, o_ang, o_un, o_bb4, o_rg4, o_pred);
-}
+  resnet_tail_kernel<<<32, 128, 0, stream>>>(
+      s_cur, s_init,
+      ps_arwin, ps_arwinit, ar_bin, ar_binit,
+      ps_arw1, ar_b1, ps_arw2, ar_b2,
+      ar_wout, ar_bout, w_bb, b_bb,
+      aatype, def_frames, group_idx, atom_mask, lit_pos,
+      o_ang, o_un, o_bb4, o_rg4, o_pred);
+}
```

After: 1.409 ms. 1.28x slower.
